# Kernel tuning notes

Hardware: AMD Instinct MI355X
Metric: run time of the kernel (lower is better)

The kernel has to match this reference:

```python
import jax, jax.numpy as jnp
import numpy as np

K = 16          # gcn_k
NHEAD = 4
C = 256         # feat_dims
EPS = 1e-5
LAYERS = ('gcn', 'cross_attn', 'gcn', 'cross_attn')


def _inorm(x, axes):
    # torch InstanceNorm (affine=False): normalize per (batch, channel) over spatial axes
    mu = jnp.mean(x, axes, keepdims=True)
    var = jnp.var(x, axes, keepdims=True)
    return (x - mu) * jax.lax.rsqrt(var + EPS)


def _lrelu(x):
    return jnp.where(x >= 0, x, 0.2 * x)


def _conv1d(x, W, b=None):
    # 1x1 Conv1d: x (B,Cin,N), W (Cout,Cin)
    y = jnp.einsum('bcn,oc->bon', x, W)
    return y if b is None else y + b[None, :, None]


def _graph_features(feats, coords, k):
    # feats (B,N,Cf), coords (B,N,3) -> (B,N,k,2Cf)  [EdgeConv features]
    sq = jnp.sum(coords * coords, axis=-1)  # (B,N)
    d = sq[:, :, None] + sq[:, None, :] - 2.0 * jnp.einsum('bnc,bmc->bnm', coords, coords)
    _, inds = jax.lax.top_k(-d, k + 1)       # k+1 smallest distances, sorted
    inds = inds[:, :, 1:]                    # drop self
    neigh = jax.vmap(lambda f, i: f[i])(feats, inds)  # (B,N,k,Cf)
    center = jnp.broadcast_to(feats[:, :, None, :], neigh.shape)
    return jnp.concatenate([center, neigh - center], axis=-1)


def _gcn(coords, feats, W1, W2, W3, k):
    # coords (B,3,N), feats (B,C,N) -> (B,C,N)
    c = jnp.transpose(coords, (0, 2, 1))
    f = jnp.transpose(feats, (0, 2, 1))
    g1 = _graph_features(f, c, k)                                   # (B,N,k,2C)
    h1 = _lrelu(_inorm(jnp.einsum('bnkc,oc->bonk', g1, W1), (2, 3)))
    f1 = jnp.max(h1, axis=-1)                                       # (B,C,N)
    g2 = _graph_features(jnp.transpose(f1, (0, 2, 1)), c, k)        # (B,N,k,2C)
    h2 = _lrelu(_inorm(jnp.einsum('bnkc,oc->bonk', g2, W2), (2, 3)))
    f2 = jnp.max(h2, axis=-1)                                       # (B,2C,N)
    f3 = jnp.concatenate([feats, f1, f2], axis=1)                   # (B,4C,N)
    return _lrelu(_inorm(_conv1d(f3, W3), (2,)))


def _cross_attn(f1, f2, Wq, bq, Wk, bk, Wv, bv, Wo, bo, Wm1, bm1, Wm2, bm2, nhead):
    B, Cc, N = f1.shape
    d = Cc // nhead
    # torch reshape (B, C, N) -> (B, d, nhead, N): channel c = dd*nhead + h
    q = _conv1d(f1, Wq, bq).reshape(B, d, nhead, -1)
    k = _conv1d(f2, Wk, bk).reshape(B, d, nhead, -1)
    v = _conv1d(f2, Wv, bv).reshape(B, d, nhead, -1)
    scores = jnp.einsum('bdhn,bdhm->bhnm', q, k) / (d ** 0.5)
    attn = jax.nn.softmax(scores, axis=-1)
    feats = jnp.einsum('bhnm,bdhm->bdhn', attn, v).reshape(B, Cc, -1)
    feats = _conv1d(feats, Wo, bo)
    h = _conv1d(jnp.concatenate([f1, feats], axis=1), Wm1, bm1)
    h = jax.nn.relu(_inorm(h, (2,)))
    return _conv1d(h, Wm2, bm2)


def _forward(coords1, feats1, coords2, feats2, gcn_W1, gcn_W2, gcn_W3, ca):
    for li, name in enumerate(LAYERS):
        i = li // 2  # index into stacked per-block params
        if name == 'gcn':
            feats1 = _gcn(coords1, feats1, gcn_W1[i], gcn_W2[i], gcn_W3[i], K)
            feats2 = _gcn(coords2, feats2, gcn_W1[i], gcn_W2[i], gcn_W3[i], K)
        else:
            p = tuple(t[i] for t in ca)
            feats1 = _cross_attn(feats1, feats2, *p, NHEAD)
            feats2 = _cross_attn(feats2, feats1, *p, NHEAD)
    return feats1, feats2


def setup_inputs() -> dict:
    key = jax.random.key(0)
    ks = jax.random.split(key, 20)
    B, N, M = 2, 2048, 2048
    s = 0.05
    f32 = jnp.float32
    return {
        'coords1': jax.random.normal(ks[0], (B, 3, N), f32),
        'feats1': jax.random.normal(ks[1], (B, C, N), f32),
        'coords2': jax.random.normal(ks[2], (B, 3, M), f32),
        'feats2': jax.random.normal(ks[3], (B, C, M), f32),
        'gcn_W1': jax.random.normal(ks[4], (2, C, 2 * C), f32) * s,
        'gcn_W2': jax.random.normal(ks[5], (2, 2 * C, 2 * C), f32) * s,
        'gcn_W3': jax.random.normal(ks[6], (2, C, 4 * C), f32) * s,
        'ca_Wq': jax.random.normal(ks[7], (2, C, C), f32) * s,
        'ca_bq': jax.random.normal(ks[8], (2, C), f32) * s,
        'ca_Wk': jax.random.normal(ks[9], (2, C, C), f32) * s,
        'ca_bk': jax.random.normal(ks[10], (2, C), f32) * s,
        'ca_Wv': jax.random.normal(ks[11], (2, C, C), f32) * s,
        'ca_bv': jax.random.normal(ks[12], (2, C), f32) * s,
        'ca_Wo': jax.random.normal(ks[13], (2, C, C), f32) * s,
        'ca_bo': jax.random.normal(ks[14], (2, C), f32) * s,
        'ca_Wm1': jax.random.normal(ks[15], (2, 2 * C, 2 * C), f32) * s,
        'ca_bm1': jax.random.normal(ks[16], (2, 2 * C), f32) * s,
        'ca_Wm2': jax.random.normal(ks[17], (2, C, 2 * C), f32) * s,
        'ca_bm2': jax.random.normal(ks[18], (2, C), f32) * s,
    }


def reference(coords1, feats1, coords2, feats2, gcn_W1, gcn_W2, gcn_W3,
              ca_Wq, ca_bq, ca_Wk, ca_bk, ca_Wv, ca_bv, ca_Wo, ca_bo,
              ca_Wm1, ca_bm1, ca_Wm2, ca_bm2):
    ca = (ca_Wq, ca_bq, ca_Wk, ca_bk, ca_Wv, ca_bv, ca_Wo, ca_bo,
          ca_Wm1, ca_bm1, ca_Wm2, ca_bm2)
    return _forward(coords1, feats1, coords2, feats2, gcn_W1, gcn_W2, gcn_W3, ca)
```

## Files before the change

### kernel.cpp

```cpp
#include <hip/hip_runtime.h>


namespace {

constexpr int BB = 2, NPV = 2048, CCH = 256, KNB = 16;
typedef long long i64;
typedef unsigned short u16;
typedef unsigned int u32;
constexpr i64 NSTR  = (i64)NPV * 256;
constexpr i64 NSTR2 = (i64)NPV * 512;
constexpr i64 NSTR4 = (i64)NPV * 1024;
constexpr i64 MB = 1048576;

typedef __attribute__((ext_vector_type(8))) short short8v;
typedef __attribute__((ext_vector_type(4))) float f32x4;

__device__ __forceinline__ float lrelu(float v) { return v >= 0.f ? v : 0.2f * v; }

__device__ __forceinline__ void splitbf(float x, u16& h, u16& l) {
  unsigned u = __float_as_uint(x);
  h = (u16)(u >> 16);
  float hf = __uint_as_float(u & 0xffff0000u);
  l = (u16)(__float_as_uint(x - hf) >> 16);
}

__device__ __forceinline__ u16 f2bf_rn(float x) {
  u32 u = __float_as_uint(x);
  return (u16)((u + 0x7fffu + ((u >> 16) & 1u)) >> 16);
}
__device__ __forceinline__ float bf2f(u16 h) {
  return __uint_as_float((u32)h << 16);
}

__global__ __launch_bounds__(256) void k_diag(float* out, int n, float v) {
  int i = blockIdx.x * 256 + threadIdx.x;
  if (i < n) out[i] = v;
}

__global__ __launch_bounds__(256) void k_setup(
    const float* __restrict__ fa, const float* __restrict__ fb,
    float* __restrict__ Xa, float* __restrict__ Xb,
    const float* __restrict__ W1b, const float* __restrict__ W2b,
    float* __restrict__ UVS,
    const float* __restrict__ Wob, float* __restrict__ WoT,
    const float* __restrict__ Wm1b_, float* __restrict__ Wfull,
    const float* __restrict__ bm1b_, const float* __restrict__ bob,
    float* __restrict__ bcomb) {
  int blk = blockIdx.x;
  int t = threadIdx.x;
  if (blk < 8192) {
    int gi = blk * 256 + t;
    bool second = gi >= (1 << 20);
    int idx = gi & ((1 << 20) - 1);
    int b = idx >> 19;
    int n = (idx >> 8) & (NPV - 1);
    int c = idx & (CCH - 1);
    const float* f = second ? fb : fa;
    float* X = second ? Xb : Xa;
    X[idx] = f[((i64)b * CCH + c) * NPV + n];
  } else if (blk < 11264) {
    int i = (blk - 8192) * 256 + t;
    int li = i / 393216;
    int r0 = i - li * 393216;
    const float* W1 = W1b + (i64)li * 131072;
    const float* W2 = W2b + (i64)li * 262144;
    float* dst = UVS + (i64)li * 393216;
    if (r0 < 131072) {
      int r = r0 >> 8, c = r0 & 255;
      dst[r0] = (r < 256) ? W1[(i64)r * 512 + c] - W1[(i64)r * 512 + 256 + c]
                          : W1[(i64)(r - 256) * 512 + 256 + c];
    } else {
      int j = r0 - 131072;
      int r = j >> 8, c = j & 255;
      dst[131072 + j] = (r < 512) ? W2[(i64)r * 512 + c] - W2[(i64)r * 512 + 256 + c]
                                  : W2[(i64)(r - 512) * 512 + 256 + c];
    }
  } else if (blk < 11776) {
    int i = (blk - 11264) * 256 + t;
    int li = i >> 16, rem = i & 65535;
    int c = rem >> 8, k = rem & 255;
    WoT[(i64)li * 65536 + c * 256 + k] = Wob[(i64)li * 65536 + k * 256 + c];
  } else if (blk < 12800) {
    int i = (blk - 11776) * 256 + t;
    int li = i >> 17, rem = i & 131071;
    int o = rem >> 8, c = rem & 255;
    Wfull[(i64)li * 262144 + o * 512 + c] = Wm1b_[(i64)li * 262144 + o * 512 + c];
  } else {
    int g = (blk - 12800) * 256 + t;
    int li = g >> 9, o = g & 511;
    const float* wm1 = Wm1b_ + (i64)li * 262144 + (i64)o * 512 + 256;
    const float* bo = bob + (i64)li * 256;
    float acc = bm1b_[(i64)li * 512 + o];
    for (int k = 0; k < 256; k++) acc += wm1[k] * bo[k];
    bcomb[(i64)li * 512 + o] = acc;
  }
}

__global__ __launch_bounds__(1024) void k_knnp(const float* __restrict__ c1,
                                               const float* __restrict__ c2,
                                               int* __restrict__ o1,
                                               int* __restrict__ o2) {
#pragma clang fp contract(off)
  __shared__ float4 csq[NPV];
  __shared__ float md[16 * 17];
  __shared__ int   mi[16 * 17];
  int set = blockIdx.y >> 1, b = blockIdx.y & 1;
  const float* cb = (set ? c2 : c1) + (i64)b * 3 * NPV;
  int* ob = (set ? o2 : o1) + (i64)b * NPV * KNB;
  int tid = threadIdx.x;
  for (int m = tid; m < NPV; m += 1024) {
    float x = cb[m], y = cb[NPV + m], z = cb[2 * NPV + m];
    csq[m] = make_float4(x, y, z, x * x + y * y + z * z);
  }
  __syncthreads();
  int w = tid >> 6, lane = tid & 63;
  int p = w & 3, s = w >> 2;
  int n = blockIdx.x * 4 + p;
  float4 cn = csq[n];
  float xn = cn.x, yn = cn.y, zn = cn.z, sn = cn.w;
  float dc[8];
#pragma unroll
  for (int t = 0; t < 8; t++) {
    float4 c = csq[s * 512 + t * 64 + lane];
    float dot = xn * c.x + yn * c.y + zn * c.z;
    dc[t] = (sn + c.w) - 2.0f * dot;
  }
  float wd = -3.4e38f; int wm = -1;
  for (int r = 0; r < KNB + 1; r++) {
    float bd = 3.4e38f; int bm = 0x7fffffff;
#pragma unroll
    for (int t = 0; t < 8; t++) {
      int m = s * 512 + t * 64 + lane;
      float d = dc[t];
      bool valid = (d > wd) || (d == wd && m > wm);
      if (valid && (d < bd || (d == bd && m < bm))) { bd = d; bm = m; }
    }
    for (int mask = 1; mask < 64; mask <<= 1) {
      float od = __shfl_xor(bd, mask);
      int om = __shfl_xor(bm, mask);
      if (od < bd || (od == bd && om < bm)) { bd = od; bm = om; }
    }
    if (lane == 0) { md[w * 17 + r] = bd; mi[w * 17 + r] = bm; }
    wd = bd; wm = bm;
  }
  __syncthreads();
  if (w < 4) {
    int ptr = 0;
    float hd = (lane < 4) ? md[(lane * 4 + w) * 17] : 3.4e38f;
    int   hm = (lane < 4) ? mi[(lane * 4 + w) * 17] : 0x7fffffff;
    int* o = ob + (i64)(blockIdx.x * 4 + w) * KNB;
    for (int r = 0; r < KNB + 1; r++) {
      float bd = hd; int bm = hm;
      for (int mask = 1; mask < 64; mask <<= 1) {
        float od = __shfl_xor(bd, mask);
        int om = __shfl_xor(bm, mask);
        if (od < bd || (od == bd && om < bm)) { bd = od; bm = om; }
      }
      if (r > 0 && lane == 0) o[r - 1] = bm & (NPV - 1);
      if (lane < 4 && hd == bd && hm == bm) {
        ptr++;
        hd = (ptr < 17) ? md[(lane * 4 + w) * 17 + ptr] : 3.4e38f;
        hm = (ptr < 17) ? mi[(lane * 4 + w) * 17 + ptr] : 0x7fffffff;
      }
    }
  }
}

template <bool ANORM, bool ACAT, bool ESTAT, int OMODE>
__global__ __launch_bounds__(256) void k_gemm(
    const float* __restrict__ A, int lda, i64 sA,
    const float* __restrict__ A2,
    const float* __restrict__ W, int ldw, i64 sW,
    const float* __restrict__ bias,
    float* __restrict__ C, int ldc, i64 sC,
    int K, int mode, int act,
    const float* __restrict__ pin, int nchA, float invA,
    float* __restrict__ pout, int ncolsTot,
    int tmode, float* __restrict__ out2) {
  __shared__ __align__(16) u16 Ah[128][36], Al[128][36], Bh[128][36], Bl[128][36];
  __shared__ float mv[512], rv[512];
  __shared__ float cs[128][2];
  int b = blockIdx.z;
  A += (i64)b * sA;
  if (ACAT) A2 += (i64)b * NSTR;
  int m0 = blockIdx.x * 128, n0 = blockIdx.y * 128;
  int tid = threadIdx.x;
  int w = tid >> 6, l = tid & 63;
  int wr = w >> 1, wc = w & 1;
  int lc = l & 15, lq = l >> 4;
  int srow = tid >> 1, skh = (tid & 1) * 16;

  if (ANORM) {
    for (int c = tid; c < K; c += 256) {
      float s = 0.f, ss = 0.f;
      for (int hh = 0; hh < nchA; hh++) {
        s  += pin[((i64)(b * nchA + hh) * K + c) * 2];
        ss += pin[((i64)(b * nchA + hh) * K + c) * 2 + 1];
      }
      float mu = s * invA;
      mv[c] = mu;
      rv[c] = 1.0f / sqrtf(ss * invA - mu * mu + 1e-5f);
    }
    __syncthreads();
  }

  const float* Ap = A + (i64)(m0 + srow) * lda + skh;
  const float* Wp = W + (i64)b * sW + (i64)(n0 + srow) * ldw + skh;

  auto loadA = [&](int kt, float4* v) {
#pragma unroll
    for (int j = 0; j < 4; j++) {
      if (ACAT) {
        int col0 = kt + skh;
        const float* ap = (col0 < 256)
            ? A  + (i64)(m0 + srow) * 256 + col0
            : A2 + (i64)(m0 + srow) * 256 + (col0 - 256);
        v[j] = *(const float4*)(ap + j * 4);
      } else {
        v[j] = *(const float4*)(Ap + kt + j * 4);
      }
    }
  };
  auto loadW = [&](int kt, float4* v) {
#pragma unroll
    for (int j = 0; j < 4; j++) v[j] = *(const float4*)(Wp + kt + j * 4);
  };

  float4 ar[4], wv4[4];
  loadA(0, ar); loadW(0, wv4);

  f32x4 acc[4][4];
#pragma unroll
  for (int i = 0; i < 4; i++)
#pragma unroll
    for (int j = 0; j < 4; j++)
#pragma unroll
      for (int r = 0; r < 4; r++) acc[i][j][r] = 0.f;

  int koff = lq * 8;
  for (int kt = 0; kt < K; kt += 32) {
    __syncthreads();
#pragma unroll
    for (int j = 0; j < 4; j++) {
      float4 a = ar[j];
      if (ANORM) {
        float4 mu = *(const float4*)&mv[kt + skh + j * 4];
        float4 rs = *(const float4*)&rv[kt + skh + j * 4];
        a.x = (a.x - mu.x) * rs.x; a.y = (a.y - mu.y) * rs.y;
        a.z = (a.z - mu.z) * rs.z; a.w = (a.w - mu.w) * rs.w;
        if (act == 1) { a.x = lrelu(a.x); a.y = lrelu(a.y);
                        a.z = lrelu(a.z); a.w = lrelu(a.w); }
        else { a.x = fmaxf(a.x, 0.f); a.y = fmaxf(a.y, 0.f);
               a.z = fmaxf(a.z, 0.f); a.w = fmaxf(a.w, 0.f); }
      }
      u16 h0, h1, h2, h3, l0, l1, l2, l3;
      splitbf(a.x, h0, l0); splitbf(a.y, h1, l1);
      splitbf(a.z, h2, l2); splitbf(a.w, h3, l3);
      *(ushort4*)&Ah[srow][skh + j * 4] = make_ushort4(h0, h1, h2, h3);
      *(ushort4*)&Al[srow][skh + j * 4] = make_ushort4(l0, l1, l2, l3);
      float4 bb = wv4[j];
      splitbf(bb.x, h0, l0); splitbf(bb.y, h1, l1);
      splitbf(bb.z, h2, l2); splitbf(bb.w, h3, l3);
      *(ushort4*)&Bh[srow][skh + j * 4] = make_ushort4(h0, h1, h2, h3);
      *(ushort4*)&Bl[srow][skh + j * 4] = make_ushort4(l0, l1, l2, l3);
    }
    __syncthreads();
    if (kt + 32 < K) { loadA(kt + 32, ar); loadW(kt + 32, wv4); }
    short8v ah[4], al4[4], bh[4], bl4[4];
#pragma unroll
    for (int i = 0; i < 4; i++) {
      int r = wr * 64 + i * 16 + lc;
      ah[i]  = *(const short8v*)&Ah[r][koff];
      al4[i] = *(const short8v*)&Al[r][koff];
    }
#pragma unroll
    for (int j = 0; j < 4; j++) {
      int r = wc * 64 + j * 16 + lc;
      bh[j]  = *(const short8v*)&Bh[r][koff];
      bl4[j] = *(const short8v*)&Bl[r][koff];
    }
#pragma unroll
    for (int i = 0; i < 4; i++) {
#pragma unroll
      for (int j = 0; j < 4; j++) {
        acc[i][j] = __builtin_amdgcn_mfma_f32_16x16x32_bf16(ah[i], bh[j], acc[i][j], 0, 0, 0);
        acc[i][j] = __builtin_amdgcn_mfma_f32_16x16x32_bf16(al4[i], bh[j], acc[i][j], 0, 0, 0);
        acc[i][j] = __builtin_amdgcn_mfma_f32_16x16x32_bf16(ah[i], bl4[j], acc[i][j], 0, 0, 0);
      }
    }
  }

  float sj[4] = {0.f, 0.f, 0.f, 0.f}, ssj[4] = {0.f, 0.f, 0.f, 0.f};
#pragma unroll
  for (int j = 0; j < 4; j++) {
    int col = n0 + wc * 64 + j * 16 + lc;
    float bv = (mode == 0 && bias) ? bias[col] : 0.f;
#pragma unroll
    for (int i = 0; i < 4; i++) {
      int rbase = m0 + wr * 64 + i * 16 + lq * 4;
#pragma unroll
      for (int r = 0; r < 4; r++) {
        int row = rbase + r;
        float v;
        if (OMODE == 1) {
          v = acc[i][j][r];
          ((u16*)C)[(i64)b * sC + (i64)row * ldc + col] = f2bf_rn(v);
        } else {
          float* cp = &C[(i64)b * sC + (i64)row * ldc + col];
          v = acc[i][j][r] + ((mode == 0) ? bv : *cp);
          if (tmode != 2) *cp = v;
          if (tmode != 0)
            out2[(i64)b * 524288 + (i64)col * 2048 + row] = v;
        }
        if (ESTAT) { sj[j] += v; ssj[j] += v * v; }
      }
    }
  }
  if (ESTAT) {
#pragma unroll
    for (int j = 0; j < 4; j++) {
      sj[j]  += __shfl_xor(sj[j], 16);  sj[j]  += __shfl_xor(sj[j], 32);
      ssj[j] += __shfl_xor(ssj[j], 16); ssj[j] += __shfl_xor(ssj[j], 32);
    }
    __syncthreads();
    if (wr == 0 && lq == 0) {
#pragma unroll
      for (int j = 0; j < 4; j++) {
        int cl = wc * 64 + j * 16 + lc;
        cs[cl][0] = sj[j]; cs[cl][1] = ssj[j];
      }
    }
    __syncthreads();
    if (wr == 1 && lq == 0) {
#pragma unroll
      for (int j = 0; j < 4; j++) {
        int cl = wc * 64 + j * 16 + lc;
        cs[cl][0] += sj[j]; cs[cl][1] += ssj[j];
      }
    }
    __syncthreads();
    if (tid < 128) {
      i64 slot = ((i64)(b * gridDim.x + blockIdx.x) * ncolsTot + n0 + tid) * 2;
      pout[slot] = cs[tid][0];
      pout[slot + 1] = cs[tid][1];
    }
  }
}

__global__ __launch_bounds__(256) void k_qkv(
    const float* __restrict__ XA, const float* __restrict__ XB,
    const float* __restrict__ Wq, const float* __restrict__ Wk,
    const float* __restrict__ Wv,
    const float* __restrict__ bq, const float* __restrict__ bk,
    const float* __restrict__ bv,
    float* __restrict__ Qp, float* __restrict__ Kp, float* __restrict__ Vp) {
  __shared__ __align__(16) u16 Ah[128][36], Al[128][36], Bh[128][36], Bl[128][36];
  int z = blockIdx.z;
  int mat = z >> 1, b = z & 1;
  const float* A = (mat == 0 ? XA : XB) + (i64)b * NSTR;
  const float* W = (mat == 0 ? Wq : (mat == 1 ? Wk : Wv));
  const float* bias = (mat == 0 ? bq : (mat == 1 ? bk : bv));
  float* C = (mat == 0 ? Qp : (mat == 1 ? Kp : Vp)) + (i64)b * NSTR;
  int m0 = blockIdx.x * 128, n0 = blockIdx.y * 128;
  int tid = threadIdx.x;
  int w = tid >> 6, l = tid & 63;
  int wr = w >> 1, wc = w & 1;
  int lc = l & 15, lq = l >> 4;
  int srow = tid >> 1, skh = (tid & 1) * 16;
  const float* Ap = A + (i64)(m0 + srow) * 256 + skh;
  const float* Wp = W + (i64)(n0 + srow) * 256 + skh;
  float4 ar[4], wv4[4];
#pragma unroll
  for (int j = 0; j < 4; j++) { ar[j] = *(const float4*)(Ap + j * 4);
                                wv4[j] = *(const float4*)(Wp + j * 4); }
  f32x4 acc[4][4];
#pragma unroll
  for (int i = 0; i < 4; i++)
#pragma unroll
    for (int j = 0; j < 4; j++)
#pragma unroll
      for (int r = 0; r < 4; r++) acc[i][j][r] = 0.f;
  int koff = lq * 8;
  for (int kt = 0; kt < 256; kt += 32) {
    __syncthreads();
#pragma unroll
    for (int j = 0; j < 4; j++) {
      u16 h0, h1, h2, h3, l0, l1, l2, l3;
      splitbf(ar[j].x, h0, l0); splitbf(ar[j].y, h1, l1);
      splitbf(ar[j].z, h2, l2); splitbf(ar[j].w, h3, l3);
      *(ushort4*)&Ah[srow][skh + j * 4] = make_ushort4(h0, h1, h2, h3);
      *(ushort4*)&Al[srow][skh + j * 4] = make_ushort4(l0, l1, l2, l3);
      splitbf(wv4[j].x, h0, l0); splitbf(wv4[j].y, h1, l1);
      splitbf(wv4[j].z, h2, l2); splitbf(wv4[j].w, h3, l3);
      *(ushort4*)&Bh[srow][skh + j * 4] = make_ushort4(h0, h1, h2, h3);
      *(ushort4*)&Bl[srow][skh + j * 4] = make_ushort4(l0, l1, l2, l3);
    }
    __syncthreads();
    if (kt + 32 < 256) {
#pragma unroll
      for (int j = 0; j < 4; j++) { ar[j] = *(const float4*)(Ap + kt + 32 + j * 4);
                                    wv4[j] = *(const float4*)(Wp + kt + 32 + j * 4); }
    }
    short8v ah[4], al4[4], bh[4], bl4[4];
#pragma unroll
    for (int i = 0; i < 4; i++) {
      int r = wr * 64 + i * 16 + lc;
      ah[i]  = *(const short8v*)&Ah[r][koff];
      al4[i] = *(const short8v*)&Al[r][koff];
    }
#pragma unroll
    for (int j = 0; j < 4; j++) {
      int r = wc * 64 + j * 16 + lc;
      bh[j]  = *(const short8v*)&Bh[r][koff];
      bl4[j] = *(const short8v*)&Bl[r][koff];
    }
#pragma unroll
    for (int i = 0; i < 4; i++)
#pragma unroll
      for (int j = 0; j < 4; j++) {
        acc[i][j] = __builtin_amdgcn_mfma_f32_16x16x32_bf16(ah[i], bh[j], acc[i][j], 0, 0, 0);
        acc[i][j] = __builtin_amdgcn_mfma_f32_16x16x32_bf16(al4[i], bh[j], acc[i][j], 0, 0, 0);
        acc[i][j] = __builtin_amdgcn_mfma_f32_16x16x32_bf16(ah[i], bl4[j], acc[i][j], 0, 0, 0);
      }
  }
#pragma unroll
  for (int j = 0; j < 4; j++) {
    int col = n0 + wc * 64 + j * 16 + lc;
    float bv = bias[col];
#pragma unroll
    for (int i = 0; i < 4; i++) {
      int rbase = m0 + wr * 64 + i * 16 + lq * 4;
#pragma unroll
      for (int r = 0; r < 4; r++) {
        float v = acc[i][j][r] + bv;
        int row = rbase + r;
        if (mat == 0) C[(i64)row * 256 + col] = v;
        else C[((i64)(col & 3) * 2048 + row) * 64 + (col >> 2)] = v;
      }
    }
  }
}

__global__ __launch_bounds__(256) void k_y3(
    const float* __restrict__ Xbase, const float* __restrict__ F1b,
    const float* __restrict__ F2b, const float* __restrict__ W3b,
    float* __restrict__ Cb,
    const float* __restrict__ pA, const float* __restrict__ pB,
    float* __restrict__ pout, int li) {
  __shared__ __align__(16) u16 Ah[128][36], Al[128][36], Bh[128][36], Bl[128][36];
  __shared__ float mv[1024], rv[1024];
  __shared__ float cs[128][2];
  int z = blockIdx.z;
  const float* X = Xbase + (i64)z * NSTR;
  const float* F1 = F1b + (i64)z * NSTR;
  const float* F2 = F2b + (i64)z * NSTR2;
  const float* W3 = W3b + (i64)li * 262144;
  float* C = Cb + (i64)z * NSTR;
  int m0 = blockIdx.x * 128, n0 = blockIdx.y * 128;
  int tid = threadIdx.x;
  int w = tid >> 6, l = tid & 63;
  int wr = w >> 1, wc = w & 1;
  int lc = l & 15, lq = l >> 4;
  int srow = tid >> 1, skh = (tid & 1) * 16;
  for (int c = tid; c < 768; c += 256) {
    int col = 256 + c;
    const float* P; int cols, idx;
    if (col < 512) { P = pA; cols = 256; idx = col - 256; }
    else           { P = pB; cols = 512; idx = col - 512; }
    float s = 0.f, ss = 0.f;
    for (int hh = 0; hh < 64; hh++) {
      s  += P[((i64)(z * 64 + hh) * cols + idx) * 2];
      ss += P[((i64)(z * 64 + hh) * cols + idx) * 2 + 1];
    }
    float mu = s * (1.f / 32768.f);
    mv[col] = mu;
    rv[col] = 1.0f / sqrtf(ss * (1.f / 32768.f) - mu * mu + 1e-5f);
  }
  __syncthreads();
  auto loadA = [&](int kt, float4* v) {
    int col0 = kt + skh;
    const float* ap;
    if (col0 < 256)      ap = X  + (i64)(m0 + srow) * 256 + col0;
    else if (col0 < 512) ap = F1 + (i64)(m0 + srow) * 256 + (col0 - 256);
    else                 ap = F2 + (i64)(m0 + srow) * 512 + (col0 - 512);
#pragma unroll
    for (int j = 0; j < 4; j++) v[j] = *(const float4*)(ap + j * 4);
  };
  const float* Wp = W3 + (i64)(n0 + srow) * 1024 + skh;
  float4 ar[4], wv4[4];
  loadA(0, ar);
#pragma unroll
  for (int j = 0; j < 4; j++) wv4[j] = *(const float4*)(Wp + j * 4);
  f32x4 acc[4][4];
#pragma unroll
  for (int i = 0; i < 4; i++)
#pragma unroll
    for (int j = 0; j < 4; j++)
#pragma unroll
      for (int r = 0; r < 4; r++) acc[i][j][r] = 0.f;
  int koff = lq * 8;
  for (int kt = 0; kt < 1024; kt += 32) {
    __syncthreads();
    int col0 = kt + skh;
#pragma unroll
    for (int j = 0; j < 4; j++) {
      float4 a = ar[j];
      if (col0 >= 256) {
        float4 mu = *(const float4*)&mv[col0 + j * 4];
        float4 rs = *(const float4*)&rv[col0 + j * 4];
        a.x = lrelu((a.x - mu.x) * rs.x);
        a.y = lrelu((a.y - mu.y) * rs.y);
        a.z = lrelu((a.z - mu.z) * rs.z);
        a.w = lrelu((a.w - mu.w) * rs.w);
      }
      u16 h0, h1, h2, h3, l0, l1, l2, l3;
      splitbf(a.x, h0, l0); splitbf(a.y, h1, l1);
      splitbf(a.z, h2, l2); splitbf(a.w, h3, l3);
      *(ushort4*)&Ah[srow][skh + j * 4] = make_ushort4(h0, h1, h2, h3);
      *(ushort4*)&Al[srow][skh + j * 4] = make_ushort4(l0, l1, l2, l3);
      splitbf(wv4[j].x, h0, l0); splitbf(wv4[j].y, h1, l1);
      splitbf(wv4[j].z, h2, l2); splitbf(wv4[j].w, h3, l3);
      *(ushort4*)&Bh[srow][skh + j * 4] = make_ushort4(h0, h1, h2, h3);
      *(ushort4*)&Bl[srow][skh + j * 4] = make_ushort4(l0, l1, l2, l3);
    }
    __syncthreads();
    if (kt + 32 < 1024) {
      loadA(kt + 32, ar);
#pragma unroll
      for (int j = 0; j < 4; j++) wv4[j] = *(const float4*)(Wp + kt + 32 + j * 4);
    }
    short8v ah[4], al4[4], bh[4], bl4[4];
#pragma unroll
    for (int i = 0; i < 4; i++) {
      int r = wr * 64 + i * 16 + lc;
      ah[i]  = *(const short8v*)&Ah[r][koff];
      al4[i] = *(const short8v*)&Al[r][koff];
    }
#pragma unroll
    for (int j = 0; j < 4; j++) {
      int r = wc * 64 + j * 16 + lc;
      bh[j]  = *(const short8v*)&Bh[r][koff];
      bl4[j] = *(const short8v*)&Bl[r][koff];
    }
#pragma unroll
    for (int i = 0; i < 4; i++)
#pragma unroll
      for (int j = 0; j < 4; j++) {
        acc[i][j] = __builtin_amdgcn_mfma_f32_16x16x32_bf16(ah[i], bh[j], acc[i][j], 0, 0, 0);
        acc[i][j] = __builtin_amdgcn_mfma_f32_16x16x32_bf16(al4[i], bh[j], acc[i][j], 0, 0, 0);
        acc[i][j] = __builtin_amdgcn_mfma_f32_16x16x32_bf16(ah[i], bl4[j], acc[i][j], 0, 0, 0);
      }
  }
  float sj[4] = {0.f, 0.f, 0.f, 0.f}, ssj[4] = {0.f, 0.f, 0.f, 0.f};
#pragma unroll
  for (int j = 0; j < 4; j++) {
    int col = n0 + wc * 64 + j * 16 + lc;
#pragma unroll
    for (int i = 0; i < 4; i++) {
      int rbase = m0 + wr * 64 + i * 16 + lq * 4;
#pragma unroll
      for (int r = 0; r < 4; r++) {
        float v = acc[i][j][r];
        C[(i64)(rbase + r) * 256 + col] = v;
        sj[j] += v; ssj[j] += v * v;
      }
    }
  }
#pragma unroll
  for (int j = 0; j < 4; j++) {
    sj[j]  += __shfl_xor(sj[j], 16);  sj[j]  += __shfl_xor(sj[j], 32);
    ssj[j] += __shfl_xor(ssj[j], 16); ssj[j] += __shfl_xor(ssj[j], 32);
  }
  __syncthreads();
  if (wr == 0 && lq == 0) {
#pragma unroll
    for (int j = 0; j < 4; j++) {
      int cl = wc * 64 + j * 16 + lc;
      cs[cl][0] = sj[j]; cs[cl][1] = ssj[j];
    }
  }
  __syncthreads();
  if (wr == 1 && lq == 0) {
#pragma unroll
    for (int j = 0; j < 4; j++) {
      int cl = wc * 64 + j * 16 + lc;
      cs[cl][0] += sj[j]; cs[cl][1] += ssj[j];
    }
  }
  __syncthreads();
  if (tid < 128) {
    i64 slot = ((i64)(z * 16 + blockIdx.x) * 256 + n0 + tid) * 2;
    pout[slot] = cs[tid][0];
    pout[slot + 1] = cs[tid][1];
  }
}

template <bool BF16IN>
__global__ __launch_bounds__(256) void k_gstat(const void* __restrict__ Pv,
                                               const void* __restrict__ Qv,
                                               int ldpq,
                                               const int* __restrict__ knn,
                                               int O, float* __restrict__ RM,
                                               float* __restrict__ part) {
  int b = blockIdx.z;
  int o = blockIdx.x * 256 + threadIdx.x;
  int n0 = blockIdx.y * 32;
  RM += (i64)b * 2048 * O;
  knn += ((i64)b * 2048 + n0) * KNB;
  __shared__ int js[32 * KNB];
  for (int i = threadIdx.x; i < 32 * KNB; i += 256) js[i] = knn[i];
  __syncthreads();
  i64 base = (i64)b * 2048 * ldpq;
  float s = 0.f, ss = 0.f;
  for (int r = 0; r < 32; r++) {
    int n = n0 + r;
    float p = BF16IN ? bf2f(((const u16*)Pv)[base + (i64)n * ldpq + o])
                     : ((const float*)Pv)[base + (i64)n * ldpq + o];
    float qm = -3.4e38f, qs = 0.f, qss = 0.f;
#pragma unroll
    for (int k = 0; k < KNB; k++) {
      i64 qoff = base + (i64)js[r * KNB + k] * ldpq + o;
      float q = BF16IN ? bf2f(((const u16*)Qv)[qoff]) : ((const float*)Qv)[qoff];
      qm = fmaxf(qm, q); qs += q; qss += q * q;
    }
    RM[(i64)n * O + o] = p + qm;
    s  += 16.f * p + qs;
    ss += 16.f * p * p + 2.f * p * qs + qss;
  }
  i64 slot = ((i64)b * 64 + blockIdx.y) * O + o;
  part[slot * 2] = s; part[slot * 2 + 1] = ss;
}

__global__ __launch_bounds__(256) void k_normP(const float* __restrict__ src,
                                               float* __restrict__ dst, int cols,
                                               const float* __restrict__ part,
                                               int nch, float inv, int act) {
  int b = blockIdx.z;
  i64 n = blockIdx.x;
  int c = blockIdx.y * 256 + threadIdx.x;
  float s = 0.f, ss = 0.f;
  for (int h = 0; h < nch; h++) {
    s  += part[((i64)(b * nch + h) * cols + c) * 2];
    ss += part[((i64)(b * nch + h) * cols + c) * 2 + 1];
  }
  float mu = s * inv;
  float rs = 1.0f / sqrtf(ss * inv - mu * mu + 1e-5f);
  i64 off = ((i64)b * 2048 + n) * cols + c;
  float v = (src[off] - mu) * rs;
  dst[off] = (act == 1) ? lrelu(v) : fmaxf(v, 0.f);
}

__global__ __launch_bounds__(256) void k_flash(const float* __restrict__ Qp,
                                               const float* __restrict__ Kp,
                                               const float* __restrict__ Vp,
                                               float* __restrict__ Op) {
  __shared__ __align__(16) u16 Kh[64][76], Kl[64][76];
  __shared__ __align__(16) u16 Vh[64][76], Vl[64][76];
  __shared__ __align__(16) u16 Ph[4][16][76], Pl[4][16][76];
  int qt = blockIdx.x, h = blockIdx.y, b = blockIdx.z;
  const float* Qb = Qp + (i64)b * NSTR;
  const float* Khm = Kp + (i64)b * NSTR + (i64)h * 131072;
  const float* Vhm = Vp + (i64)b * NSTR + (i64)h * 131072;
  int tid = threadIdx.x;
  int w = tid >> 6, l = tid & 63;
  int lc = l & 15, lq = l >> 4;
  short8v qh[2], ql[2];
  int qrow = qt * 64 + w * 16 + lc;
#pragma unroll
  for (int ks = 0; ks < 2; ks++) {
#pragma unroll
    for (int j = 0; j < 8; j++) {
      float v = Qb[(i64)qrow * 256 + 4 * (ks * 32 + lq * 8 + j) + h];
      u16 hh, ll; splitbf(v, hh, ll);
      qh[ks][j] = (short)hh; ql[ks][j] = (short)ll;
    }
  }
  float m_r[4] = {-3.0e38f, -3.0e38f, -3.0e38f, -3.0e38f};
  float l_r[4] = {0.f, 0.f, 0.f, 0.f};
  f32x4 acc[4];
#pragma unroll
  for (int j = 0; j < 4; j++)
#pragma unroll
    for (int r = 0; r < 4; r++) acc[j][r] = 0.f;

  for (int kt = 0; kt < 32; kt++) {
    __syncthreads();
    {
      const float* Kt = Khm + (i64)kt * 4096;
      const float* Vt = Vhm + (i64)kt * 4096;
#pragma unroll
      for (int q = 0; q < 4; q++) {
        int v = q * 256 + tid;
        int m = v >> 4, d4 = (v & 15) * 4;
        u16 h0, h1, h2, h3, l0, l1, l2, l3;
        float4 kf = *(const float4*)(Kt + (i64)v * 4);
        splitbf(kf.x, h0, l0); splitbf(kf.y, h1, l1);
        splitbf(kf.z, h2, l2); splitbf(kf.w, h3, l3);
        *(ushort4*)&Kh[m][d4] = make_ushort4(h0, h1, h2, h3);
        *(ushort4*)&Kl[m][d4] = make_ushort4(l0, l1, l2, l3);
        float4 vf = *(const float4*)(Vt + (i64)v * 4);
        splitbf(vf.x, h0, l0); splitbf(vf.y, h1, l1);
        splitbf(vf.z, h2, l2); splitbf(vf.w, h3, l3);
        Vh[d4 + 0][m] = h0; Vh[d4 + 1][m] = h1;
        Vh[d4 + 2][m] = h2; Vh[d4 + 3][m] = h3;
        Vl[d4 + 0][m] = l0; Vl[d4 + 1][m] = l1;
        Vl[d4 + 2][m] = l2; Vl[d4 + 3][m] = l3;
      }
    }
    __syncthreads();
    f32x4 s[4];
#pragma unroll
    for (int j = 0; j < 4; j++)
#pragma unroll
      for (int r = 0; r < 4; r++) s[j][r] = 0.f;
#pragma unroll
    for (int ks = 0; ks < 2; ks++) {
      int ko = ks * 32 + lq * 8;
#pragma unroll
      for (int j = 0; j < 4; j++) {
        short8v bh = *(const short8v*)&Kh[j * 16 + lc][ko];
        short8v bl = *(const short8v*)&Kl[j * 16 + lc][ko];
        s[j] = __builtin_amdgcn_mfma_f32_16x16x32_bf16(qh[ks], bh, s[j], 0, 0, 0);
        s[j] = __builtin_amdgcn_mfma_f32_16x16x32_bf16(ql[ks], bh, s[j], 0, 0, 0);
        s[j] = __builtin_amdgcn_mfma_f32_16x16x32_bf16(qh[ks], bl, s[j], 0, 0, 0);
      }
    }
#pragma unroll
    for (int j = 0; j < 4; j++)
#pragma unroll
      for (int r = 0; r < 4; r++) s[j][r] *= 0.125f;
    float rmax[4];
#pragma unroll
    for (int r = 0; r < 4; r++)
      rmax[r] = fmaxf(fmaxf(s[0][r], s[1][r]), fmaxf(s[2][r], s[3][r]));
#pragma unroll
    for (int mask = 1; mask < 16; mask <<= 1)
#pragma unroll
      for (int r = 0; r < 4; r++) rmax[r] = fmaxf(rmax[r], __shfl_xor(rmax[r], mask));
    float fs[4], rsum[4];
#pragma unroll
    for (int r = 0; r < 4; r++) {
      float mn = fmaxf(m_r[r], rmax[r]);
      fs[r] = expf(m_r[r] - mn);
      m_r[r] = mn; rsum[r] = 0.f;
    }
#pragma unroll
    for (int j = 0; j < 4; j++)
#pragma unroll
      for (int r = 0; r < 4; r++) {
        float p = expf(s[j][r] - m_r[r]);
        rsum[r] += p;
        u16 hh, ll; splitbf(p, hh, ll);
        Ph[w][lq * 4 + r][j * 16 + lc] = hh;
        Pl[w][lq * 4 + r][j * 16 + lc] = ll;
      }
#pragma unroll
    for (int mask = 1; mask < 16; mask <<= 1)
#pragma unroll
      for (int r = 0; r < 4; r++) rsum[r] += __shfl_xor(rsum[r], mask);
#pragma unroll
    for (int r = 0; r < 4; r++) l_r[r] = l_r[r] * fs[r] + rsum[r];
#pragma unroll
    for (int j = 0; j < 4; j++)
#pragma unroll
      for (int r = 0; r < 4; r++) acc[j][r] *= fs[r];
#pragma unroll
    for (int ks = 0; ks < 2; ks++) {
      int ko = ks * 32 + lq * 8;
      short8v ph = *(const short8v*)&Ph[w][lc][ko];
      short8v pl = *(const short8v*)&Pl[w][lc][ko];
#pragma unroll
      for (int j = 0; j < 4; j++) {
        short8v bh = *(const short8v*)&Vh[j * 16 + lc][ko];
        short8v bl = *(const short8v*)&Vl[j * 16 + lc][ko];
        acc[j] = __builtin_amdgcn_mfma_f32_16x16x32_bf16(ph, bh, acc[j], 0, 0, 0);
        acc[j] = __builtin_amdgcn_mfma_f32_16x16x32_bf16(pl, bh, acc[j], 0, 0, 0);
        acc[j] = __builtin_amdgcn_mfma_f32_16x16x32_bf16(ph, bl, acc[j], 0, 0, 0);
      }
    }
  }
  float* Ob = Op + (i64)b * NSTR;
#pragma unroll
  for (int j = 0; j < 4; j++) {
    int dd = j * 16 + lc;
#pragma unroll
    for (int r = 0; r < 4; r++) {
      int q = qt * 64 + w * 16 + lq * 4 + r;
      Ob[(i64)q * 256 + 4 * dd + h] = acc[j][r] / l_r[r];
    }
  }
}

}

extern "C" void kernel_launch(void* const* d_in, const int* in_sizes, int n_in,
                              void* d_out, int out_size, void* d_ws, size_t ws_size,
                              hipStream_t stream) {
  float* outp = (float*)d_out;
  auto diag = [&](float v) {
    k_diag<<<dim3((out_size + 255) / 256), dim3(256), 0, stream>>>(outp, out_size, v);
  };

  static const int DSZ[19] = {12288, 1048576, 12288, 1048576, 262144, 524288, 524288,
                              131072, 512, 131072, 512, 131072, 512, 131072, 512,
                              524288, 1024, 262144, 512};
  if (n_in != 19) { diag(1000.f + (float)n_in); return; }
  for (int i = 0; i < 19; i++) {
    if (in_sizes[i] != DSZ[i]) { diag(2000.f + (float)i); return; }
  }
  if (out_size != 2097152) { diag(3000.f); return; }
  constexpr size_t NEED = 50331648;
  if (ws_size < NEED) { diag((float)(ws_size >> 20)); return; }

  char* w = (char*)d_ws;
  float* S0 = (float*)(w + 0);
  float* S1 = (float*)(w + 4 * MB);
  int*   KN1 = (int*)(w + 8 * MB);
  int*   KN2 = (int*)(w + 8 * MB + 262144);
  float* PARTA = (float*)(w + 8912896);
  float* PARTB = (float*)(w + 9437184);
  float* PARTCg = (float*)(w + 10485760);
  float* PARTCa = (float*)(w + 10616832);
  float* BCOMB = (float*)(w + 10747904);
  float* UVS   = (float*)(w + 10752000);
  float* WFULL = (float*)(w + 13897728);
  char* AR = w + 15994880;

  float* WOT = (float*)(AR + 24 * MB);
  float* PQ1 = (float*)(AR);
  u16*   PQ2 = (u16*)(AR);
  float* F2  = (float*)(AR + 16 * MB);
  float* Y3  = (float*)(AR);
  float* F1d = (float*)d_out;
  float* Qp = (float*)(AR);
  float* Kp = (float*)(AR + 4 * MB);
  float* Vp = (float*)(AR + 8 * MB);
  float* Oc = (float*)(AR + 12 * MB);
  float* Hh = (float*)(AR + 16 * MB);

  const float* W1b = (const float*)d_in[4];
  const float* W2b = (const float*)d_in[5];
  const float* W3b = (const float*)d_in[6];
  const float* Wqb = (const float*)d_in[7];   const float* bqb = (const float*)d_in[8];
  const float* Wkb = (const float*)d_in[9];   const float* bkb = (const float*)d_in[10];
  const float* Wvb = (const float*)d_in[11];  const float* bvb = (const float*)d_in[12];
  const float* Wob = (const float*)d_in[13];  const float* bob = (const float*)d_in[14];
  const float* Wm1b = (const float*)d_in[15]; const float* bm1b = (const float*)d_in[16];
  const float* Wm2b = (const float*)d_in[17]; const float* bm2b = (const float*)d_in[18];

  k_knnp<<<dim3(NPV / 4, 4), dim3(1024), 0, stream>>>(
      (const float*)d_in[0], (const float*)d_in[2], KN1, KN2);
  k_setup<<<dim3(12804), dim3(256), 0, stream>>>(
      (const float*)d_in[1], (const float*)d_in[3], S0, S1,
      W1b, W2b, UVS, Wob, WOT, Wm1b, WFULL, bm1b, bob, BCOMB);
  k_gemm<false, false, false, 0><<<dim3(4, 2, 2), dim3(256), 0, stream>>>(
      Wm1b + 256, 512, 262144, nullptr, WOT, 256, 65536, nullptr,
      WFULL + 256, 512, 262144, 256, 0, 0, nullptr, 0, 0.f, nullptr, 0,
      0, nullptr);

  auto gcn = [&](int li) {
    const float* UV1 = UVS + (i64)li * 393216;
    const float* UV2 = UVS + (i64)li * 393216 + 131072;
    k_gemm<false, false, false, 0><<<dim3(16, 4, 4), dim3(256), 0, stream>>>(
        S0, 256, NSTR, nullptr, UV1, 256, 0, nullptr, PQ1, 512, NSTR2, 256, 0, 0,
        nullptr, 0, 0.f, nullptr, 0, 0, nullptr);
    k_gstat<false><<<dim3(1, 64, 4), dim3(256), 0, stream>>>(
        PQ1, PQ1 + 256, 512, KN1, 256, F1d, PARTA);
    k_gemm<true, false, false, 1><<<dim3(16, 8, 4), dim3(256), 0, stream>>>(
        F1d, 256, NSTR, nullptr, UV2, 256, 0, nullptr,
        (float*)PQ2, 1024, NSTR4, 256, 0, 1,
        PARTA, 64, 1.f / 32768.f, nullptr, 0, 0, nullptr);
    k_gstat<true><<<dim3(2, 64, 4), dim3(256), 0, stream>>>(
        PQ2, PQ2 + 512, 1024, KN1, 512, F2, PARTB);
    k_y3<<<dim3(16, 2, 4), dim3(256), 0, stream>>>(S0, F1d, F2, W3b, Y3,
                                                   PARTA, PARTB, PARTCg, li);
    k_normP<<<dim3(2048, 1, 4), dim3(256), 0, stream>>>(Y3, S0, 256, PARTCg, 16,
                                                        1.f / 2048.f, 1);
  };

  auto attn = [&](const float* XA, const float* XB, float* XO, int li,
                  int tmode, float* out2) {
    const float* Wq = Wqb + (i64)li * 65536;   const float* bq = bqb + (i64)li * 256;
    const float* Wk = Wkb + (i64)li * 65536;   const float* bk = bkb + (i64)li * 256;
    const float* Wv = Wvb + (i64)li * 65536;   const float* bv = bvb + (i64)li * 256;
    const float* Wm2 = Wm2b + (i64)li * 131072; const float* bm2 = bm2b + (i64)li * 256;
    k_qkv<<<dim3(16, 2, 6), dim3(256), 0, stream>>>(XA, XB, Wq, Wk, Wv,
                                                    bq, bk, bv, Qp, Kp, Vp);
    k_flash<<<dim3(32, 4, BB), dim3(256), 0, stream>>>(Qp, Kp, Vp, Oc);
    k_gemm<false, true, true, 0><<<dim3(16, 4, 2), dim3(256), 0, stream>>>(
        XA, 256, NSTR, Oc, WFULL + (i64)li * 262144, 512, 0,
        BCOMB + (i64)li * 512, Hh, 512, NSTR2, 512, 0, 0,
        nullptr, 0, 0.f, PARTCa, 512, 0, nullptr);
    k_gemm<true, false, false, 0><<<dim3(16, 2, 2), dim3(256), 0, stream>>>(
        Hh, 512, NSTR2, nullptr, Wm2, 512, 0, bm2, XO, 256, NSTR, 512, 0, 2,
        PARTCa, 16, 1.f / 2048.f, nullptr, 0, tmode, out2);
  };

  gcn(0);
  attn(S0, S1, S0, 0, 0, nullptr);
  attn(S1, S0, S1, 0, 0, nullptr);
  gcn(1);
  attn(S0, S1, S0, 1, 1, outp);
  attn(S1, S0, S1, 1, 2, outp + 1048576);
}
```

Baseline: 1.495 ms.

## Fuse per-layer kernel chains into persistent megakernels with software grid barriers

Each GCN layer's six kernel launches and each cross-attention layer's four launches are merged into one 256-block persistent kernel. The stages are separated by a global atomic-counter grid barrier, with counters zeroed in the setup kernel. The goal is to remove launch gaps and per-kernel tail effects on the many small launches in the pipeline. In exchange, work is capped at 256 blocks, so stages that previously used 512 blocks run serially per block. The barrier also relies on all blocks being co-resident, which risks deadlock or a timeout break if they are not.

```diff
diff --git a/kernel.cpp b/kernel.cpp
--- a/kernel.cpp
+++ b/kernel.cpp
@@ -32,6 +32,33 @@
   return __uint_as_float((u32)h << 16);
 }
 
+__device__ __forceinline__ void gridbar(unsigned* bar, unsigned target) {
+  __syncthreads();
+  if (threadIdx.x == 0) {
+    __threadfence();
+    atomicAdd(bar, 1u);
+    int guard = 0;
+    while (atomicAdd(bar, 0u) < target) {
+      __builtin_amdgcn_s_sleep(2);
+      if (++guard > (1 << 24)) break;
+    }
+    __threadfence();
+  }
+  __syncthreads();
+}
+
+struct SmemG {
+  u16 Ah[128][36], Al[128][36], Bh[128][36], Bl[128][36];
+  float mv[1024], rv[1024];
+  float cs[128][2];
+};
+struct SmemF {
+  u16 Kh[64][76], Kl[64][76], Vh[64][76], Vl[64][76];
+  u16 Ph[4][16][76], Pl[4][16][76];
+};
+constexpr size_t SMEM_MAX = sizeof(SmemF) > sizeof(SmemG) ? sizeof(SmemF)
+                                                          : sizeof(SmemG);
+
 __global__ __launch_bounds__(256) void k_diag(float* out, int n, float v) {
   int i = blockIdx.x * 256 + threadIdx.x;
   if (i < n) out[i] = v;
@@ -45,7 +72,7 @@
     const float* __restrict__ Wob, float* __restrict__ WoT,
     const float* __restrict__ Wm1b_, float* __restrict__ Wfull,
     const float* __restrict__ bm1b_, const float* __restrict__ bob,
-    float* __restrict__ bcomb) {
+    float* __restrict__ bcomb, unsigned* __restrict__ BAR) {
   int blk = blockIdx.x;
   int t = threadIdx.x;
   if (blk < 8192) {
@@ -87,6 +114,7 @@
     Wfull[(i64)li * 262144 + o * 512 + c] = Wm1b_[(i64)li * 262144 + o * 512 + c];
   } else {
     int g = (blk - 12800) * 256 + t;
+    if (g < 16) BAR[g] = 0u;
     int li = g >> 9, o = g & 511;
     const float* wm1 = Wm1b_ + (i64)li * 262144 + (i64)o * 512 + 256;
     const float* bo = bob + (i64)li * 256;
@@ -167,23 +195,16 @@
 }
 
 template <bool ANORM, bool ACAT, bool ESTAT, int OMODE>
-__global__ __launch_bounds__(256) void k_gemm(
-    const float* __restrict__ A, int lda, i64 sA,
-    const float* __restrict__ A2,
-    const float* __restrict__ W, int ldw, i64 sW,
-    const float* __restrict__ bias,
-    float* __restrict__ C, int ldc, i64 sC,
-    int K, int mode, int act,
-    const float* __restrict__ pin, int nchA, float invA,
-    float* __restrict__ pout, int ncolsTot,
-    int tmode, float* __restrict__ out2) {
-  __shared__ __align__(16) u16 Ah[128][36], Al[128][36], Bh[128][36], Bl[128][36];
-  __shared__ float mv[512], rv[512];
-  __shared__ float cs[128][2];
-  int b = blockIdx.z;
+__device__ void dev_gemm(SmemG& S, int bx, int by, int b, int gx,
+    const float* A, int lda, i64 sA, const float* A2,
+    const float* W, int ldw, i64 sW, const float* bias,
+    float* C, int ldc, i64 sC, int K, int mode, int act,
+    const float* pin, int nchA, float invA,
+    float* pout, int ncolsTot, int tmode, float* out2) {
+  __syncthreads();
   A += (i64)b * sA;
   if (ACAT) A2 += (i64)b * NSTR;
-  int m0 = blockIdx.x * 128, n0 = blockIdx.y * 128;
+  int m0 = bx * 128, n0 = by * 128;
   int tid = threadIdx.x;
   int w = tid >> 6, l = tid & 63;
   int wr = w >> 1, wc = w & 1;
@@ -198,8 +219,8 @@
         ss += pin[((i64)(b * nchA + hh) * K + c) * 2 + 1];
       }
       float mu = s * invA;
-      mv[c] = mu;
-      rv[c] = 1.0f / sqrtf(ss * invA - mu * mu + 1e-5f);
+      S.mv[c] = mu;
+      S.rv[c] = 1.0f / sqrtf(ss * invA - mu * mu + 1e-5f);
     }
     __syncthreads();
   }
@@ -244,8 +265,8 @@
     for (int j = 0; j < 4; j++) {
       float4 a = ar[j];
       if (ANORM) {
-        float4 mu = *(const float4*)&mv[kt + skh + j * 4];
-        float4 rs = *(const float4*)&rv[kt + skh + j * 4];
+        float4 mu = *(const float4*)&S.mv[kt + skh + j * 4];
+        float4 rs = *(const float4*)&S.rv[kt + skh + j * 4];
         a.x = (a.x - mu.x) * rs.x; a.y = (a.y - mu.y) * rs.y;
         a.z = (a.z - mu.z) * rs.z; a.w = (a.w - mu.w) * rs.w;
         if (act == 1) { a.x = lrelu(a.x); a.y = lrelu(a.y);
@@ -256,13 +277,13 @@
       u16 h0, h1, h2, h3, l0, l1, l2, l3;
       splitbf(a.x, h0, l0); splitbf(a.y, h1, l1);
       splitbf(a.z, h2, l2); splitbf(a.w, h3, l3);
-      *(ushort4*)&Ah[srow][skh + j * 4] = make_ushort4(h0, h1, h2, h3);
-      *(ushort4*)&Al[srow][skh + j * 4] = make_ushort4(l0, l1, l2, l3);
+      *(ushort4*)&S.Ah[srow][skh + j * 4] = make_ushort4(h0, h1, h2, h3);
+      *(ushort4*)&S.Al[srow][skh + j * 4] = make_ushort4(l0, l1, l2, l3);
       float4 bb = wv4[j];
       splitbf(bb.x, h0, l0); splitbf(bb.y, h1, l1);
       splitbf(bb.z, h2, l2); splitbf(bb.w, h3, l3);
-      *(ushort4*)&Bh[srow][skh + j * 4] = make_ushort4(h0, h1, h2, h3);
-      *(ushort4*)&Bl[srow][skh + j * 4] = make_ushort4(l0, l1, l2, l3);
+      *(ushort4*)&S.Bh[srow][skh + j * 4] = make_ushort4(h0, h1, h2, h3);
+      *(ushort4*)&S.Bl[srow][skh + j * 4] = make_ushort4(l0, l1, l2, l3);
     }
     __syncthreads();
     if (kt + 32 < K) { loadA(kt + 32, ar); loadW(kt + 32, wv4); }
@@ -270,14 +291,14 @@
 #pragma unroll
     for (int i = 0; i < 4; i++) {
       int r = wr * 64 + i * 16 + lc;
-      ah[i]  = *(const short8v*)&Ah[r][koff];
-      al4[i] = *(const short8v*)&Al[r][koff];
+      ah[i]  = *(const short8v*)&S.Ah[r][koff];
+      al4[i] = *(const short8v*)&S.Al[r][koff];
     }
 #pragma unroll
     for (int j = 0; j < 4; j++) {
       int r = wc * 64 + j * 16 + lc;
-      bh[j]  = *(const short8v*)&Bh[r][koff];
-      bl4[j] = *(const short8v*)&Bl[r][koff];
+      bh[j]  = *(const short8v*)&S.Bh[r][koff];
+      bl4[j] = *(const short8v*)&S.Bl[r][koff];
     }
 #pragma unroll
     for (int i = 0; i < 4; i++) {
@@ -327,7 +348,7 @@
 #pragma unroll
       for (int j = 0; j < 4; j++) {
         int cl = wc * 64 + j * 16 + lc;
-        cs[cl][0] = sj[j]; cs[cl][1] = ssj[j];
+        S.cs[cl][0] = sj[j]; S.cs[cl][1] = ssj[j];
       }
     }
     __syncthreads();
@@ -335,33 +356,30 @@
 #pragma unroll
       for (int j = 0; j < 4; j++) {
         int cl = wc * 64 + j * 16 + lc;
-        cs[cl][0] += sj[j]; cs[cl][1] += ssj[j];
+        S.cs[cl][0] += sj[j]; S.cs[cl][1] += ssj[j];
       }
     }
     __syncthreads();
     if (tid < 128) {
-      i64 slot = ((i64)(b * gridDim.x + blockIdx.x) * ncolsTot + n0 + tid) * 2;
-      pout[slot] = cs[tid][0];
-      pout[slot + 1] = cs[tid][1];
-    }
-  }
-}
-
-__global__ __launch_bounds__(256) void k_qkv(
-    const float* __restrict__ XA, const float* __restrict__ XB,
-    const float* __restrict__ Wq, const float* __restrict__ Wk,
-    const float* __restrict__ Wv,
-    const float* __restrict__ bq, const float* __restrict__ bk,
-    const float* __restrict__ bv,
-    float* __restrict__ Qp, float* __restrict__ Kp, float* __restrict__ Vp) {
-  __shared__ __align__(16) u16 Ah[128][36], Al[128][36], Bh[128][36], Bl[128][36];
-  int z = blockIdx.z;
+      i64 slot = ((i64)(b * gx + bx) * ncolsTot + n0 + tid) * 2;
+      pout[slot] = S.cs[tid][0];
+      pout[slot + 1] = S.cs[tid][1];
+    }
+  }
+}
+
+__device__ void dev_qkv(SmemG& S, int bx, int by, int z,
+    const float* XA, const float* XB,
+    const float* Wq, const float* Wk, const float* Wv,
+    const float* bq, const float* bk, const float* bv,
+    float* Qp, float* Kp, float* Vp) {
+  __syncthreads();
   int mat = z >> 1, b = z & 1;
   const float* A = (mat == 0 ? XA : XB) + (i64)b * NSTR;
   const float* W = (mat == 0 ? Wq : (mat == 1 ? Wk : Wv));
   const float* bias = (mat == 0 ? bq : (mat == 1 ? bk : bv));
   float* C = (mat == 0 ? Qp : (mat == 1 ? Kp : Vp)) + (i64)b * NSTR;
-  int m0 = blockIdx.x * 128, n0 = blockIdx.y * 128;
+  int m0 = bx * 128, n0 = by * 128;
   int tid = threadIdx.x;
   int w = tid >> 6, l = tid & 63;
   int wr = w >> 1, wc = w & 1;
@@ -388,12 +406,12 @@
       u16 h0, h1, h2, h3, l0, l1, l2, l3;
       splitbf(ar[j].x, h0, l0); splitbf(ar[j].y, h1, l1);
       splitbf(ar[j].z, h2, l2); splitbf(ar[j].w, h3, l3);
-      *(ushort4*)&Ah[srow][skh + j * 4] = make_ushort4(h0, h1, h2, h3);
-      *(ushort4*)&Al[srow][skh + j * 4] = make_ushort4(l0, l1, l2, l3);
+      *(ushort4*)&S.Ah[srow][skh + j * 4] = make_ushort4(h0, h1, h2, h3);
+      *(ushort4*)&S.Al[srow][skh + j * 4] = make_ushort4(l0, l1, l2, l3);
       splitbf(wv4[j].x, h0, l0); splitbf(wv4[j].y, h1, l1);
       splitbf(wv4[j].z, h2, l2); splitbf(wv4[j].w, h3, l3);
-      *(ushort4*)&Bh[srow][skh + j * 4] = make_ushort4(h0, h1, h2, h3);
-      *(ushort4*)&Bl[srow][skh + j * 4] = make_ushort4(l0, l1, l2, l3);
+      *(ushort4*)&S.Bh[srow][skh + j * 4] = make_ushort4(h0, h1, h2, h3);
+      *(ushort4*)&S.Bl[srow][skh + j * 4] = make_ushort4(l0, l1, l2, l3);
     }
     __syncthreads();
     if (kt + 32 < 256) {
@@ -405,14 +423,14 @@
 #pragma unroll
     for (int i = 0; i < 4; i++) {
       int r = wr * 64 + i * 16 + lc;
-      ah[i]  = *(const short8v*)&Ah[r][koff];
-      al4[i] = *(const short8v*)&Al[r][koff];
+      ah[i]  = *(const short8v*)&S.Ah[r][koff];
+      al4[i] = *(const short8v*)&S.Al[r][koff];
     }
 #pragma unroll
     for (int j = 0; j < 4; j++) {
       int r = wc * 64 + j * 16 + lc;
-      bh[j]  = *(const short8v*)&Bh[r][koff];
-      bl4[j] = *(const short8v*)&Bl[r][koff];
+      bh[j]  = *(const short8v*)&S.Bh[r][koff];
+      bl4[j] = *(const short8v*)&S.Bl[r][koff];
     }
 #pragma unroll
     for (int i = 0; i < 4; i++)
@@ -441,22 +459,151 @@
   }
 }
 
-__global__ __launch_bounds__(256) void k_y3(
-    const float* __restrict__ Xbase, const float* __restrict__ F1b,
-    const float* __restrict__ F2b, const float* __restrict__ W3b,
-    float* __restrict__ Cb,
-    const float* __restrict__ pA, const float* __restrict__ pB,
-    float* __restrict__ pout, int li) {
-  __shared__ __align__(16) u16 Ah[128][36], Al[128][36], Bh[128][36], Bl[128][36];
-  __shared__ float mv[1024], rv[1024];
-  __shared__ float cs[128][2];
-  int z = blockIdx.z;
+__device__ void dev_flash(SmemF& S, int qt, int h, int b,
+    const float* Qp, const float* Kp, const float* Vp, float* Op) {
+  __syncthreads();
+  const float* Qb = Qp + (i64)b * NSTR;
+  const float* Khm = Kp + (i64)b * NSTR + (i64)h * 131072;
+  const float* Vhm = Vp + (i64)b * NSTR + (i64)h * 131072;
+  int tid = threadIdx.x;
+  int w = tid >> 6, l = tid & 63;
+  int lc = l & 15, lq = l >> 4;
+  short8v qh[2], ql[2];
+  int qrow = qt * 64 + w * 16 + lc;
+#pragma unroll
+  for (int ks = 0; ks < 2; ks++) {
+#pragma unroll
+    for (int j = 0; j < 8; j++) {
+      float v = Qb[(i64)qrow * 256 + 4 * (ks * 32 + lq * 8 + j) + h];
+      u16 hh, ll; splitbf(v, hh, ll);
+      qh[ks][j] = (short)hh; ql[ks][j] = (short)ll;
+    }
+  }
+  float m_r[4] = {-3.0e38f, -3.0e38f, -3.0e38f, -3.0e38f};
+  float l_r[4] = {0.f, 0.f, 0.f, 0.f};
+  f32x4 acc[4];
+#pragma unroll
+  for (int j = 0; j < 4; j++)
+#pragma unroll
+    for (int r = 0; r < 4; r++) acc[j][r] = 0.f;
+
+  for (int kt = 0; kt < 32; kt++) {
+    __syncthreads();
+    {
+      const float* Kt = Khm + (i64)kt * 4096;
+      const float* Vt = Vhm + (i64)kt * 4096;
+#pragma unroll
+      for (int q = 0; q < 4; q++) {
+        int v = q * 256 + tid;
+        int m = v >> 4, d4 = (v & 15) * 4;
+        u16 h0, h1, h2, h3, l0, l1, l2, l3;
+        float4 kf = *(const float4*)(Kt + (i64)v * 4);
+        splitbf(kf.x, h0, l0); splitbf(kf.y, h1, l1);
+        splitbf(kf.z, h2, l2); splitbf(kf.w, h3, l3);
+        *(ushort4*)&S.Kh[m][d4] = make_ushort4(h0, h1, h2, h3);
+        *(ushort4*)&S.Kl[m][d4] = make_ushort4(l0, l1, l2, l3);
+        float4 vf = *(const float4*)(Vt + (i64)v * 4);
+        splitbf(vf.x, h0, l0); splitbf(vf.y, h1, l1);
+        splitbf(vf.z, h2, l2); splitbf(vf.w, h3, l3);
+        S.Vh[d4 + 0][m] = h0; S.Vh[d4 + 1][m] = h1;
+        S.Vh[d4 + 2][m] = h2; S.Vh[d4 + 3][m] = h3;
+        S.Vl[d4 + 0][m] = l0; S.Vl[d4 + 1][m] = l1;
+        S.Vl[d4 + 2][m] = l2; S.Vl[d4 + 3][m] = l3;
+      }
+    }
+    __syncthreads();
+    f32x4 s[4];
+#pragma unroll
+    for (int j = 0; j < 4; j++)
+#pragma unroll
+      for (int r = 0; r < 4; r++) s[j][r] = 0.f;
+#pragma unroll
+    for (int ks = 0; ks < 2; ks++) {
+      int ko = ks * 32 + lq * 8;
+#pragma unroll
+      for (int j = 0; j < 4; j++) {
+        short8v bh = *(const short8v*)&S.Kh[j * 16 + lc][ko];
+        short8v bl = *(const short8v*)&S.Kl[j * 16 + lc][ko];
+        s[j] = __builtin_amdgcn_mfma_f32_16x16x32_bf16(qh[ks], bh, s[j], 0, 0, 0);
+        s[j] = __builtin_amdgcn_mfma_f32_16x16x32_bf16(ql[ks], bh, s[j], 0, 0, 0);
+        s[j] = __builtin_amdgcn_mfma_f32_16x16x32_bf16(qh[ks], bl, s[j], 0, 0, 0);
+      }
+    }
+#pragma unroll
+    for (int j = 0; j < 4; j++)
+#pragma unroll
+      for (int r = 0; r < 4; r++) s[j][r] *= 0.125f;
+    float rmax[4];
+#pragma unroll
+    for (int r = 0; r < 4; r++)
+      rmax[r] = fmaxf(fmaxf(s[0][r], s[1][r]), fmaxf(s[2][r], s[3][r]));
+#pragma unroll
+    for (int mask = 1; mask < 16; mask <<= 1)
+#pragma unroll
+      for (int r = 0; r < 4; r++) rmax[r] = fmaxf(rmax[r], __shfl_xor(rmax[r], mask));
+    float fs[4], rsum[4];
+#pragma unroll
+    for (int r = 0; r < 4; r++) {
+      float mn = fmaxf(m_r[r], rmax[r]);
+      fs[r] = expf(m_r[r] - mn);
+      m_r[r] = mn; rsum[r] = 0.f;
+    }
+#pragma unroll
+    for (int j = 0; j < 4; j++)
+#pragma unroll
+      for (int r = 0; r < 4; r++) {
+        float p = expf(s[j][r] - m_r[r]);
+        rsum[r] += p;
+        u16 hh, ll; splitbf(p, hh, ll);
+        S.Ph[w][lq * 4 + r][j * 16 + lc] = hh;
+        S.Pl[w][lq * 4 + r][j * 16 + lc] = ll;
+      }
+#pragma unroll
+    for (int mask = 1; mask < 16; mask <<= 1)
+#pragma unroll
+      for (int r = 0; r < 4; r++) rsum[r] += __shfl_xor(rsum[r], mask);
+#pragma unroll
+    for (int r = 0; r < 4; r++) l_r[r] = l_r[r] * fs[r] + rsum[r];
+#pragma unroll
+    for (int j = 0; j < 4; j++)
+#pragma unroll
+      for (int r = 0; r < 4; r++) acc[j][r] *= fs[r];
+#pragma unroll
+    for (int ks = 0; ks < 2; ks++) {
+      int ko = ks * 32 + lq * 8;
+      short8v ph = *(const short8v*)&S.Ph[w][lc][ko];
+      short8v pl = *(const short8v*)&S.Pl[w][lc][ko];
+#pragma unroll
+      for (int j = 0; j < 4; j++) {
+        short8v bh = *(const short8v*)&S.Vh[j * 16 + lc][ko];
+        short8v bl = *(const short8v*)&S.Vl[j * 16 + lc][ko];
+        acc[j] = __builtin_amdgcn_mfma_f32_16x16x32_bf16(ph, bh, acc[j], 0, 0, 0);
+        acc[j] = __builtin_amdgcn_mfma_f32_16x16x32_bf16(pl, bh, acc[j], 0, 0, 0);
+        acc[j] = __builtin_amdgcn_mfma_f32_16x16x32_bf16(ph, bl, acc[j], 0, 0, 0);
+      }
+    }
+  }
+  float* Ob = Op + (i64)b * NSTR;
+#pragma unroll
+  for (int j = 0; j < 4; j++) {
+    int dd = j * 16 + lc;
+#pragma unroll
+    for (int r = 0; r < 4; r++) {
+      int q = qt * 64 + w * 16 + lq * 4 + r;
+      Ob[(i64)q * 256 + 4 * dd + h] = acc[j][r] / l_r[r];
+    }
+  }
+}
+
+__device__ void dev_y3(SmemG& S, int bx, int by, int z,
+    const float* Xbase, const float* F1b, const float* F2b, const float* W3,
+    float* Cb, const float* pA, const float* pB, float* pout) {
+  __syncthreads();
   const float* X = Xbase + (i64)z * NSTR;
   const float* F1 = F1b + (i64)z * NSTR;
   const float* F2 = F2b + (i64)z * NSTR2;
-  const float* W3 = W3b + (i64)li * 262144;
   float* C = Cb + (i64)z * NSTR;
-  int m0 = blockIdx.x * 128, n0 = blockIdx.y * 128;
+  int m0 = bx * 128, n0 = by * 128;
   int tid = threadIdx.x;
   int w = tid >> 6, l = tid & 63;
   int wr = w >> 1, wc = w & 1;
@@ -473,8 +620,8 @@
       ss += P[((i64)(z * 64 + hh) * cols + idx) * 2 + 1];
     }
     float mu = s * (1.f / 32768.f);
-    mv[col] = mu;
-    rv[col] = 1.0f / sqrtf(ss * (1.f / 32768.f) - mu * mu + 1e-5f);
+    S.mv[col] = mu;
+    S.rv[col] = 1.0f / sqrtf(ss * (1.f / 32768.f) - mu * mu + 1e-5f);
   }
   __syncthreads();
   auto loadA = [&](int kt, float4* v) {
@@ -506,8 +653,8 @@
     for (int j = 0; j < 4; j++) {
       float4 a = ar[j];
       if (col0 >= 256) {
-        float4 mu = *(const float4*)&mv[col0 + j * 4];
-        float4 rs = *(const float4*)&rv[col0 + j * 4];
+        float4 mu = *(const float4*)&S.mv[col0 + j * 4];
+        float4 rs = *(const float4*)&S.rv[col0 + j * 4];
         a.x = lrelu((a.x - mu.x) * rs.x);
         a.y = lrelu((a.y - mu.y) * rs.y);
         a.z = lrelu((a.z - mu.z) * rs.z);
@@ -516,12 +663,12 @@
       u16 h0, h1, h2, h3, l0, l1, l2, l3;
       splitbf(a.x, h0, l0); splitbf(a.y, h1, l1);
       splitbf(a.z, h2, l2); splitbf(a.w, h3, l3);
-      *(ushort4*)&Ah[srow][skh + j * 4] = make_ushort4(h0, h1, h2, h3);
-      *(ushort4*)&Al[srow][skh + j * 4] = make_ushort4(l0, l1, l2, l3);
+      *(ushort4*)&S.Ah[srow][skh + j * 4] = make_ushort4(h0, h1, h2, h3);
+      *(ushort4*)&S.Al[srow][skh + j * 4] = make_ushort4(l0, l1, l2, l3);
       splitbf(wv4[j].x, h0, l0); splitbf(wv4[j].y, h1, l1);
       splitbf(wv4[j].z, h2, l2); splitbf(wv4[j].w, h3, l3);
-      *(ushort4*)&Bh[srow][skh + j * 4] = make_ushort4(h0, h1, h2, h3);
-      *(ushort4*)&Bl[srow][skh + j * 4] = make_ushort4(l0, l1, l2, l3);
+      *(ushort4*)&S.Bh[srow][skh + j * 4] = make_ushort4(h0, h1, h2, h3);
+      *(ushort4*)&S.Bl[srow][skh + j * 4] = make_ushort4(l0, l1, l2, l3);
     }
     __syncthreads();
     if (kt + 32 < 1024) {
@@ -533,14 +680,14 @@
 #pragma unroll
     for (int i = 0; i < 4; i++) {
       int r = wr * 64 + i * 16 + lc;
-      ah[i]  = *(const short8v*)&Ah[r][koff];
-      al4[i] = *(const short8v*)&Al[r][koff];
+      ah[i]  = *(const short8v*)&S.Ah[r][koff];
+      al4[i] = *(const short8v*)&S.Al[r][koff];
     }
 #pragma unroll
     for (int j = 0; j < 4; j++) {
       int r = wc * 64 + j * 16 + lc;
-      bh[j]  = *(const short8v*)&Bh[r][koff];
-      bl4[j] = *(const short8v*)&Bl[r][koff];
+      bh[j]  = *(const short8v*)&S.Bh[r][koff];
+      bl4[j] = *(const short8v*)&S.Bl[r][koff];
     }
 #pragma unroll
     for (int i = 0; i < 4; i++)
@@ -576,7 +723,7 @@
 #pragma unroll
     for (int j = 0; j < 4; j++) {
       int cl = wc * 64 + j * 16 + lc;
-      cs[cl][0] = sj[j]; cs[cl][1] = ssj[j];
+      S.cs[cl][0] = sj[j]; S.cs[cl][1] = ssj[j];
     }
   }
   __syncthreads();
@@ -584,30 +731,26 @@
 #pragma unroll
     for (int j = 0; j < 4; j++) {
       int cl = wc * 64 + j * 16 + lc;
-      cs[cl][0] += sj[j]; cs[cl][1] += ssj[j];
+      S.cs[cl][0] += sj[j]; S.cs[cl][1] += ssj[j];
     }
   }
   __syncthreads();
   if (tid < 128) {
-    i64 slot = ((i64)(z * 16 + blockIdx.x) * 256 + n0 + tid) * 2;
-    pout[slot] = cs[tid][0];
-    pout[slot + 1] = cs[tid][1];
+    i64 slot = ((i64)(z * 16 + bx) * 256 + n0 + tid) * 2;
+    pout[slot] = S.cs[tid][0];
+    pout[slot + 1] = S.cs[tid][1];
   }
 }
 
 template <bool BF16IN>
-__global__ __launch_bounds__(256) void k_gstat(const void* __restrict__ Pv,
-                                               const void* __restrict__ Qv,
-                                               int ldpq,
-                                               const int* __restrict__ knn,
-                                               int O, float* __restrict__ RM,
-                                               float* __restrict__ part) {
-  int b = blockIdx.z;
-  int o = blockIdx.x * 256 + threadIdx.x;
-  int n0 = blockIdx.y * 32;
+__device__ void dev_gstat(int* js, int bx, int by, int b,
+    const void* Pv, const void* Qv, int ldpq, const int* knn,
+    int O, float* RM, float* part) {
+  __syncthreads();
+  int o = bx * 256 + threadIdx.x;
+  int n0 = by * 32;
   RM += (i64)b * 2048 * O;
   knn += ((i64)b * 2048 + n0) * KNB;
-  __shared__ int js[32 * KNB];
   for (int i = threadIdx.x; i < 32 * KNB; i += 256) js[i] = knn[i];
   __syncthreads();
   i64 base = (i64)b * 2048 * ldpq;
@@ -627,168 +770,119 @@
     s  += 16.f * p + qs;
     ss += 16.f * p * p + 2.f * p * qs + qss;
   }
-  i64 slot = ((i64)b * 64 + blockIdx.y) * O + o;
+  i64 slot = ((i64)b * 64 + by) * O + o;
   part[slot * 2] = s; part[slot * 2 + 1] = ss;
 }
 
-__global__ __launch_bounds__(256) void k_normP(const float* __restrict__ src,
-                                               float* __restrict__ dst, int cols,
-                                               const float* __restrict__ part,
-                                               int nch, float inv, int act) {
-  int b = blockIdx.z;
-  i64 n = blockIdx.x;
-  int c = blockIdx.y * 256 + threadIdx.x;
+__device__ void dev_normP(SmemG& S, int z, int rc,
+    const float* src, float* dst, const float* part) {
+  __syncthreads();
+  int c = threadIdx.x;
   float s = 0.f, ss = 0.f;
-  for (int h = 0; h < nch; h++) {
-    s  += part[((i64)(b * nch + h) * cols + c) * 2];
-    ss += part[((i64)(b * nch + h) * cols + c) * 2 + 1];
-  }
-  float mu = s * inv;
-  float rs = 1.0f / sqrtf(ss * inv - mu * mu + 1e-5f);
-  i64 off = ((i64)b * 2048 + n) * cols + c;
-  float v = (src[off] - mu) * rs;
-  dst[off] = (act == 1) ? lrelu(v) : fmaxf(v, 0.f);
-}
-
-__global__ __launch_bounds__(256) void k_flash(const float* __restrict__ Qp,
-                                               const float* __restrict__ Kp,
-                                               const float* __restrict__ Vp,
-                                               float* __restrict__ Op) {
-  __shared__ __align__(16) u16 Kh[64][76], Kl[64][76];
-  __shared__ __align__(16) u16 Vh[64][76], Vl[64][76];
-  __shared__ __align__(16) u16 Ph[4][16][76], Pl[4][16][76];
-  int qt = blockIdx.x, h = blockIdx.y, b = blockIdx.z;
-  const float* Qb = Qp + (i64)b * NSTR;
-  const float* Khm = Kp + (i64)b * NSTR + (i64)h * 131072;
-  const float* Vhm = Vp + (i64)b * NSTR + (i64)h * 131072;
-  int tid = threadIdx.x;
-  int w = tid >> 6, l = tid & 63;
-  int lc = l & 15, lq = l >> 4;
-  short8v qh[2], ql[2];
-  int qrow = qt * 64 + w * 16 + lc;
-#pragma unroll
-  for (int ks = 0; ks < 2; ks++) {
-#pragma unroll
-    for (int j = 0; j < 8; j++) {
-      float v = Qb[(i64)qrow * 256 + 4 * (ks * 32 + lq * 8 + j) + h];
-      u16 hh, ll; splitbf(v, hh, ll);
-      qh[ks][j] = (short)hh; ql[ks][j] = (short)ll;
-    }
-  }
-  float m_r[4] = {-3.0e38f, -3.0e38f, -3.0e38f, -3.0e38f};
-  float l_r[4] = {0.f, 0.f, 0.f, 0.f};
-  f32x4 acc[4];
-#pragma unroll
-  for (int j = 0; j < 4; j++)
-#pragma unroll
-    for (int r = 0; r < 4; r++) acc[j][r] = 0.f;
-
-  for (int kt = 0; kt < 32; kt++) {
-    __syncthreads();
-    {
-      const float* Kt = Khm + (i64)kt * 4096;
-      const float* Vt = Vhm + (i64)kt * 4096;
-#pragma unroll
-      for (int q = 0; q < 4; q++) {
-        int v = q * 256 + tid;
-        int m = v >> 4, d4 = (v & 15) * 4;
-        u16 h0, h1, h2, h3, l0, l1, l2, l3;
-        float4 kf = *(const float4*)(Kt + (i64)v * 4);
-        splitbf(kf.x, h0, l0); splitbf(kf.y, h1, l1);
-        splitbf(kf.z, h2, l2); splitbf(kf.w, h3, l3);
-        *(ushort4*)&Kh[m][d4] = make_ushort4(h0, h1, h2, h3);
-        *(ushort4*)&Kl[m][d4] = make_ushort4(l0, l1, l2, l3);
-        float4 vf = *(const float4*)(Vt + (i64)v * 4);
-        splitbf(vf.x, h0, l0); splitbf(vf.y, h1, l1);
-        splitbf(vf.z, h2, l2); splitbf(vf.w, h3, l3);
-        Vh[d4 + 0][m] = h0; Vh[d4 + 1][m] = h1;
-        Vh[d4 + 2][m] = h2; Vh[d4 + 3][m] = h3;
-        Vl[d4 + 0][m] = l0; Vl[d4 + 1][m] = l1;
-        Vl[d4 + 2][m] = l2; Vl[d4 + 3][m] = l3;
-      }
-    }
-    __syncthreads();
-    f32x4 s[4];
-#pragma unroll
-    for (int j = 0; j < 4; j++)
-#pragma unroll
-      for (int r = 0; r < 4; r++) s[j][r] = 0.f;
-#pragma unroll
-    for (int ks = 0; ks < 2; ks++) {
-      int ko = ks * 32 + lq * 8;
-#pragma unroll
-      for (int j = 0; j < 4; j++) {
-        short8v bh = *(const short8v*)&Kh[j * 16 + lc][ko];
-        short8v bl = *(const short8v*)&Kl[j * 16 + lc][ko];
-        s[j] = __builtin_amdgcn_mfma_f32_16x16x32_bf16(qh[ks], bh, s[j], 0, 0, 0);
-        s[j] = __builtin_amdgcn_mfma_f32_16x16x32_bf16(ql[ks], bh, s[j], 0, 0, 0);
-        s[j] = __builtin_amdgcn_mfma_f32_16x16x32_bf16(qh[ks], bl, s[j], 0, 0, 0);
-      }
-    }
-#pragma unroll
-    for (int j = 0; j < 4; j++)
-#pragma unroll
-      for (int r = 0; r < 4; r++) s[j][r] *= 0.125f;
-    float rmax[4];
-#pragma unroll
-    for (int r = 0; r < 4; r++)
-      rmax[r] = fmaxf(fmaxf(s[0][r], s[1][r]), fmaxf(s[2][r], s[3][r]));
-#pragma unroll
-    for (int mask = 1; mask < 16; mask <<= 1)
-#pragma unroll
-      for (int r = 0; r < 4; r++) rmax[r] = fmaxf(rmax[r], __shfl_xor(rmax[r], mask));
-    float fs[4], rsum[4];
-#pragma unroll
-    for (int r = 0; r < 4; r++) {
-      float mn = fmaxf(m_r[r], rmax[r]);
-      fs[r] = expf(m_r[r] - mn);
-      m_r[r] = mn; rsum[r] = 0.f;
-    }
-#pragma unroll
-    for (int j = 0; j < 4; j++)
-#pragma unroll
-      for (int r = 0; r < 4; r++) {
-        float p = expf(s[j][r] - m_r[r]);
-        rsum[r] += p;
-        u16 hh, ll; splitbf(p, hh, ll);
-        Ph[w][lq * 4 + r][j * 16 + lc] = hh;
-        Pl[w][lq * 4 + r][j * 16 + lc] = ll;
-      }
-#pragma unroll
-    for (int mask = 1; mask < 16; mask <<= 1)
-#pragma unroll
-      for (int r = 0; r < 4; r++) rsum[r] += __shfl_xor(rsum[r], mask);
-#pragma unroll
-    for (int r = 0; r < 4; r++) l_r[r] = l_r[r] * fs[r] + rsum[r];
-#pragma unroll
-    for (int j = 0; j < 4; j++)
-#pragma unroll
-      for (int r = 0; r < 4; r++) acc[j][r] *= fs[r];
-#pragma unroll
-    for (int ks = 0; ks < 2; ks++) {
-      int ko = ks * 32 + lq * 8;
-      short8v ph = *(const short8v*)&Ph[w][lc][ko];
-      short8v pl = *(const short8v*)&Pl[w][lc][ko];
-#pragma unroll
-      for (int j = 0; j < 4; j++) {
-        short8v bh = *(const short8v*)&Vh[j * 16 + lc][ko];
-        short8v bl = *(const short8v*)&Vl[j * 16 + lc][ko];
-        acc[j] = __builtin_amdgcn_mfma_f32_16x16x32_bf16(ph, bh, acc[j], 0, 0, 0);
-        acc[j] = __builtin_amdgcn_mfma_f32_16x16x32_bf16(pl, bh, acc[j], 0, 0, 0);
-        acc[j] = __builtin_amdgcn_mfma_f32_16x16x32_bf16(ph, bl, acc[j], 0, 0, 0);
-      }
-    }
-  }
-  float* Ob = Op + (i64)b * NSTR;
-#pragma unroll
-  for (int j = 0; j < 4; j++) {
-    int dd = j * 16 + lc;
-#pragma unroll
-    for (int r = 0; r < 4; r++) {
-      int q = qt * 64 + w * 16 + lq * 4 + r;
-      Ob[(i64)q * 256 + 4 * dd + h] = acc[j][r] / l_r[r];
-    }
-  }
+  for (int h = 0; h < 16; h++) {
+    s  += part[((i64)(z * 16 + h) * 256 + c) * 2];
+    ss += part[((i64)(z * 16 + h) * 256 + c) * 2 + 1];
+  }
+  float mu = s * (1.f / 2048.f);
+  S.mv[c] = mu;
+  S.rv[c] = 1.0f / sqrtf(ss * (1.f / 2048.f) - mu * mu + 1e-5f);
+  __syncthreads();
+  for (int r = 0; r < 32; r++) {
+    i64 row = (i64)z * 2048 + rc * 32 + r;
+    float v = (src[row * 256 + c] - S.mv[c]) * S.rv[c];
+    dst[row * 256 + c] = lrelu(v);
+  }
+}
+
+__global__ __launch_bounds__(256) void k_gcn_mega(
+    float* X, const float* UV1, const float* UV2, const float* W3,
+    const int* KN, float* PQ1, u16* PQ2, float* F2, float* Y3, float* F1d,
+    float* PARTA, float* PARTB, float* PARTCg, unsigned* bar) {
+  __shared__ __align__(16) char smem[sizeof(SmemG)];
+  SmemG& S = *(SmemG*)smem;
+  int bid = blockIdx.x;
+  {
+    int bx = bid & 15, by = (bid >> 4) & 3, z = bid >> 6;
+    dev_gemm<false, false, false, 0>(S, bx, by, z, 16,
+        X, 256, NSTR, nullptr, UV1, 256, 0, nullptr, PQ1, 512, NSTR2,
+        256, 0, 0, nullptr, 0, 0.f, nullptr, 0, 0, nullptr);
+  }
+  gridbar(bar, 256);
+  {
+    int by = bid & 63, z = bid >> 6;
+    dev_gstat<false>((int*)smem, 0, by, z, PQ1, PQ1 + 256, 512, KN, 256,
+                     F1d, PARTA);
+  }
+  gridbar(bar, 512);
+  for (int job = bid; job < 512; job += 256) {
+    int bx = job & 15, by = (job >> 4) & 7, z = job >> 7;
+    dev_gemm<true, false, false, 1>(S, bx, by, z, 16,
+        F1d, 256, NSTR, nullptr, UV2, 256, 0, nullptr, (float*)PQ2, 1024, NSTR4,
+        256, 0, 1, PARTA, 64, 1.f / 32768.f, nullptr, 0, 0, nullptr);
+  }
+  gridbar(bar, 768);
+  for (int job = bid; job < 512; job += 256) {
+    int bx = job & 1, by = (job >> 1) & 63, z = job >> 7;
+    dev_gstat<true>((int*)smem, bx, by, z, PQ2, PQ2 + 512, 1024, KN, 512,
+                    F2, PARTB);
+  }
+  gridbar(bar, 1024);
+  if (bid < 128) {
+    int bx = bid & 15, by = (bid >> 4) & 1, z = bid >> 5;
+    dev_y3(S, bx, by, z, X, F1d, F2, W3, Y3, PARTA, PARTB, PARTCg);
+  }
+  gridbar(bar, 1280);
+  {
+    int z = bid >> 6, rc = bid & 63;
+    dev_normP(S, z, rc, Y3, X, PARTCg);
+  }
+}
+
+__global__ __launch_bounds__(256) void k_attn_mega(
+    const float* XA, const float* XB, float* XO,
+    const float* Wq, const float* Wk, const float* Wv,
+    const float* bq, const float* bk, const float* bv,
+    const float* WF, const float* BC, const float* Wm2, const float* bm2,
+    float* Qp, float* Kp, float* Vp, float* Oc, float* Hh, float* PARTCa,
+    int tmode, float* out2, unsigned* bar) {
+  __shared__ __align__(16) char smem[SMEM_MAX];
+  SmemG& SG = *(SmemG*)smem;
+  SmemF& SF = *(SmemF*)smem;
+  int bid = blockIdx.x;
+  if (bid < 192) {
+    int z = bid >> 5, rem = bid & 31;
+    int by = rem >> 4, bx = rem & 15;
+    dev_qkv(SG, bx, by, z, XA, XB, Wq, Wk, Wv, bq, bk, bv, Qp, Kp, Vp);
+  }
+  gridbar(bar, 256);
+  {
+    int qt = bid & 31, h = (bid >> 5) & 3, b = bid >> 7;
+    dev_flash(SF, qt, h, b, Qp, Kp, Vp, Oc);
+  }
+  gridbar(bar, 512);
+  if (bid < 128) {
+    int bx = bid & 15, by = (bid >> 4) & 3, b = bid >> 6;
+    dev_gemm<false, true, true, 0>(SG, bx, by, b, 16,
+        XA, 256, NSTR, Oc, WF, 512, 0, BC, Hh, 512, NSTR2,
+        512, 0, 0, nullptr, 0, 0.f, PARTCa, 512, 0, nullptr);
+  }
+  gridbar(bar, 768);
+  if (bid < 64) {
+    int bx = bid & 15, by = (bid >> 4) & 1, b = bid >> 5;
+    dev_gemm<true, false, false, 0>(SG, bx, by, b, 16,
+        Hh, 512, NSTR2, nullptr, Wm2, 512, 0, bm2, XO, 256, NSTR,
+        512, 0, 2, PARTCa, 16, 1.f / 2048.f, nullptr, 0, tmode, out2);
+  }
+}
+
+__global__ __launch_bounds__(256) void k_gemm_s(
+    const float* A, int lda, i64 sA, const float* W, int ldw, i64 sW,
+    float* C, int ldc, i64 sC, int K) {
+  __shared__ __align__(16) char smem[sizeof(SmemG)];
+  SmemG& S = *(SmemG*)smem;
+  dev_gemm<false, false, false, 0>(S, blockIdx.x, blockIdx.y, blockIdx.z,
+      gridDim.x, A, lda, sA, nullptr, W, ldw, sW, nullptr, C, ldc, sC,
+      K, 0, 0, nullptr, 0, 0.f, nullptr, 0, 0, nullptr);
 }
 
 }
@@ -824,6 +918,7 @@
   float* BCOMB = (float*)(w + 10747904);
   float* UVS   = (float*)(w + 10752000);
   float* WFULL = (float*)(w + 13897728);
+  unsigned* BAR = (unsigned*)(w + NEED - 4096);
   char* AR = w + 15994880;
 
   float* WOT = (float*)(AR + 24 * MB);
@@ -852,54 +947,32 @@
       (const float*)d_in[0], (const float*)d_in[2], KN1, KN2);
   k_setup<<<dim3(12804), dim3(256), 0, stream>>>(
       (const float*)d_in[1], (const float*)d_in[3], S0, S1,
-      W1b, W2b, UVS, Wob, WOT, Wm1b, WFULL, bm1b, bob, BCOMB);
-  k_gemm<false, false, false, 0><<<dim3(4, 2, 2), dim3(256), 0, stream>>>(
-      Wm1b + 256, 512, 262144, nullptr, WOT, 256, 65536, nullptr,
-      WFULL + 256, 512, 262144, 256, 0, 0, nullptr, 0, 0.f, nullptr, 0,
-      0, nullptr);
-
-  auto gcn = [&](int li) {
-    const float* UV1 = UVS + (i64)li * 393216;
-    const float* UV2 = UVS + (i64)li * 393216 + 131072;
-    k_gemm<false, false, false, 0><<<dim3(16, 4, 4), dim3(256), 0, stream>>>(
-        S0, 256, NSTR, nullptr, UV1, 256, 0, nullptr, PQ1, 512, NSTR2, 256, 0, 0,
-        nullptr, 0, 0.f, nullptr, 0, 0, nullptr);
-    k_gstat<false><<<dim3(1, 64, 4), dim3(256), 0, stream>>>(
-        PQ1, PQ1 + 256, 512, KN1, 256, F1d, PARTA);
-    k_gemm<true, false, false, 1><<<dim3(16, 8, 4), dim3(256), 0, stream>>>(
-        F1d, 256, NSTR, nullptr, UV2, 256, 0, nullptr,
-        (float*)PQ2, 1024, NSTR4, 256, 0, 1,
-        PARTA, 64, 1.f / 32768.f, nullptr, 0, 0, nullptr);
-    k_gstat<true><<<dim3(2, 64, 4), dim3(256), 0, stream>>>(
-        PQ2, PQ2 + 512, 1024, KN1, 512, F2, PARTB);
-    k_y3<<<dim3(16, 2, 4), dim3(256), 0, stream>>>(S0, F1d, F2, W3b, Y3,
-                                                   PARTA, PARTB, PARTCg, li);
-    k_normP<<<dim3(2048, 1, 4), dim3(256), 0, stream>>>(Y3, S0, 256, PARTCg, 16,
-                                                        1.f / 2048.f, 1);
+      W1b, W2b, UVS, Wob, WOT, Wm1b, WFULL, bm1b, bob, BCOMB, BAR);
+  k_gemm_s<<<dim3(4, 2, 2), dim3(256), 0, stream>>>(
+      Wm1b + 256, 512, 262144, WOT, 256, 65536, WFULL + 256, 512, 262144, 256);
+
+  auto gcn = [&](int li, int slot) {
+    k_gcn_mega<<<dim3(256), dim3(256), 0, stream>>>(
+        S0, UVS + (i64)li * 393216, UVS + (i64)li * 393216 + 131072,
+        W3b + (i64)li * 262144, KN1, PQ1, PQ2, F2, Y3, F1d,
+        PARTA, PARTB, PARTCg, BAR + slot);
   };
 
   auto attn = [&](const float* XA, const float* XB, float* XO, int li,
-                  int tmode, float* out2) {
-    const float* Wq = Wqb + (i64)li * 65536;   const float* bq = bqb + (i64)li * 256;
-    const float* Wk = Wkb + (i64)li * 65536;   const float* bk = bkb + (i64)li * 256;
-    const float* Wv = Wvb + (i64)li * 65536;   const float* bv = bvb + (i64)li * 256;
-    const float* Wm2 = Wm2b + (i64)li * 131072; const float* bm2 = bm2b + (i64)li * 256;
-    k_qkv<<<dim3(16, 2, 6), dim3(256), 0, stream>>>(XA, XB, Wq, Wk, Wv,
-                                                    bq, bk, bv, Qp, Kp, Vp);
-    k_flash<<<dim3(32, 4, BB), dim3(256), 0, stream>>>(Qp, Kp, Vp, Oc);
-    k_gemm<false, true, true, 0><<<dim3(16, 4, 2), dim3(256), 0, stream>>>(
-        XA, 256, NSTR, Oc, WFULL + (i64)li * 262144, 512, 0,
-        BCOMB + (i64)li * 512, Hh, 512, NSTR2, 512, 0, 0,
-        nullptr, 0, 0.f, PARTCa, 512, 0, nullptr);
-    k_gemm<true, false, false, 0><<<dim3(16, 2, 2), dim3(256), 0, stream>>>(
-        Hh, 512, NSTR2, nullptr, Wm2, 512, 0, bm2, XO, 256, NSTR, 512, 0, 2,
-        PARTCa, 16, 1.f / 2048.f, nullptr, 0, tmode, out2);
+                  int tmode, float* out2, int slot) {
+    k_attn_mega<<<dim3(256), dim3(256), 0, stream>>>(
+        XA, XB, XO,
+        Wqb + (i64)li * 65536, Wkb + (i64)li * 65536, Wvb + (i64)li * 65536,
+        bqb + (i64)li * 256, bkb + (i64)li * 256, bvb + (i64)li * 256,
+        WFULL + (i64)li * 262144, BCOMB + (i64)li * 512,
+        Wm2b + (i64)li * 131072, bm2b + (i64)li * 256,
+        Qp, Kp, Vp, Oc, Hh, PARTCa, tmode, out2, BAR + slot);
   };
 
-  gcn(0);
-  attn(S0, S1, S0, 0, 0, nullptr);
-  attn(S1, S0, S1, 0, 0, nullptr);
-  gcn(1);
-  attn(S0, S1, S0, 1, 1, outp);
-  attn(S1, S0, S1, 1, 2, outp + 1048576);
-}
+  gcn(0, 0);
+  attn(S0, S1, S0, 0, 0, nullptr, 1);
+  attn(S1, S0, S1, 0, 0, nullptr, 2);
+  gcn(1, 3);
+  attn(S0, S1, S0, 1, 1, outp, 4);
+  attn(S1, S0, S1, 1, 2, outp + 1048576, 5);
+}
```

After: 1.958 ms. 1.31x slower.
